# Optimization experiments

Hardware: AMD Instinct MI355X
Metric: run time of the kernel (lower is better)

## Reference

```python
import jax, jax.numpy as jnp
import numpy as np
from jax import lax

N = 2048    # atoms
K = 16      # knn neighbors -> E = N*K = 32768 edges
H = 128     # latent width
L = 10      # stacked InteractionNetworks
STEPS = 10  # outer simulation iterations


def _rn(key, shape, scale=0.05):
    return scale * jax.random.normal(key, shape, dtype=jnp.float32)


def setup_inputs() -> dict:
    key = jax.random.key(0)
    ks = iter(jax.random.split(key, 40))
    inp = {
        "pos": jax.random.normal(next(ks), (N, 3), dtype=jnp.float32),
        "node_f": jax.random.normal(next(ks), (N, 24), dtype=jnp.float32),
        "mass": jnp.ones((N,), jnp.float32),
        # node encoder MLP(24,128,2,128)
        "nW1": _rn(next(ks), (24, H)), "nb1": _rn(next(ks), (H,)),
        "nW2": _rn(next(ks), (H, H)), "nb2": _rn(next(ks), (H,)),
        # edge encoder MLP(4,128,2,128)
        "eW1": _rn(next(ks), (4, H)), "eb1": _rn(next(ks), (H,)),
        "eW2": _rn(next(ks), (H, H)), "eb2": _rn(next(ks), (H,)),
        # RelationModel per IN: input = 2*dim_obj + dim_rel = 384, 4 Linear layers (ReLU after each)
        "rmW1": _rn(next(ks), (L, 3 * H, H)), "rmb1": _rn(next(ks), (L, H)),
        "rmW2": _rn(next(ks), (L, H, H)), "rmb2": _rn(next(ks), (L, H)),
        "rmW3": _rn(next(ks), (L, H, H)), "rmb3": _rn(next(ks), (L, H)),
        "rmW4": _rn(next(ks), (L, H, H)), "rmb4": _rn(next(ks), (L, H)),
        # ObjectModel per IN: input = dim_obj + dim_eff = 256 -> hidden 128 -> out 128
        "omW1": _rn(next(ks), (L, 2 * H, H)), "omb1": _rn(next(ks), (L, H)),
        "omW2": _rn(next(ks), (L, H, H)), "omb2": _rn(next(ks), (L, H)),
        # decoder MLP(128,128,2,3)
        "dW1": _rn(next(ks), (H, H)), "db1": _rn(next(ks), (H,)),
        "dW2": _rn(next(ks), (H, 3)), "db2": _rn(next(ks), (3,)),
        "k": K,
    }
    return inp


def _mlp2(x, W1, b1, W2, b2):
    return jax.nn.relu(x @ W1 + b1) @ W2 + b2


def _knn_edges(pos, k):
    # knn(P.pos, k): edge_index[:,0] = sender (neighbor), edge_index[:,1] = receiver
    n = pos.shape[0]
    sq = jnp.sum(pos * pos, axis=1)
    d2 = sq[:, None] + sq[None, :] - 2.0 * (pos @ pos.T)   # [N, N]
    d2 = d2 + 1e9 * jnp.eye(n, dtype=pos.dtype)            # exclude self
    _, idx = lax.top_k(-d2, k)                              # [N, k] nearest
    senders = idx.reshape(-1)                               # [E]
    receivers = jnp.repeat(jnp.arange(n), k)                # [E]
    rel = pos[senders] - pos[receivers]
    dist = jnp.linalg.norm(rel, axis=1, keepdims=True)
    ea0 = jnp.concatenate([rel, dist], axis=1)              # [E, 4]
    return senders, receivers, ea0


def _simulate(pos, node_f, mass, nW1, nb1, nW2, nb2, eW1, eb1, eW2, eb2,
              rmW1, rmb1, rmW2, rmb2, rmW3, rmb3, rmW4, rmb4,
              omW1, omb1, omW2, omb2, dW1, db1, dW2, db2, k):
    n = pos.shape[0]
    # G.pos = G.pos + randn * 0.1 ; G.vels = zeros
    pos = pos + 0.1 * jax.random.normal(jax.random.key(42), pos.shape, dtype=pos.dtype)
    vels = jnp.zeros_like(pos)

    stacked = (rmW1, rmb1, rmW2, rmb2, rmW3, rmb3, rmW4, rmb4,
               omW1, omb1, omW2, omb2)

    for _ in range(STEPS):
        senders, receivers, ea0 = _knn_edges(pos, k)

        # encode
        x = _mlp2(node_f, nW1, nb1, nW2, nb2)    # [N, H]
        ea = _mlp2(ea0, eW1, eb1, eW2, eb2)      # [E, H]

        # process: 10 InteractionNetworks. In the original, layer(P.x, P.senders,
        # P.receivers, P.edge_attr) binds rr=senders, rs=receivers, so the
        # one-hot matmuls obj.t()@rr / obj.t()@rs are gathers by sender/receiver,
        # and e @ rr.t() is a scatter-add onto sender nodes.
        def in_step(carry, p):
            xc, eac = carry
            rW1, rb1, rW2, rb2, rW3, rb3, rW4, rb4, oW1, ob1, oW2, ob2 = p
            b = jnp.concatenate([xc[senders], xc[receivers], eac], axis=1)  # [E, 3H]
            h = jax.nn.relu(b @ rW1 + rb1)
            h = jax.nn.relu(h @ rW2 + rb2)
            h = jax.nn.relu(h @ rW3 + rb3)
            e = jax.nn.relu(h @ rW4 + rb4)                                   # [E, H]
            agg = jax.ops.segment_sum(e, senders, num_segments=n)           # e @ rr.T
            a = jnp.concatenate([xc, agg], axis=1)                           # [N, 2H]
            x_new = jax.nn.relu(a @ oW1 + ob1) @ oW2 + ob2                   # [N, H]
            return (x_new, e), None

        (x, ea), _ = lax.scan(jax.checkpoint(in_step), (x, ea), stacked)

        # decode + update
        forces = _mlp2(x, dW1, db1, dW2, db2)    # [N, 3]
        vels = vels + forces / mass[:, None]
        pos = pos + vels
    return pos


def reference(pos, node_f, mass, nW1, nb1, nW2, nb2, eW1, eb1, eW2, eb2,
              rmW1, rmb1, rmW2, rmb2, rmW3, rmb3, rmW4, rmb4,
              omW1, omb1, omW2, omb2, dW1, db1, dW2, db2, k):
    return _simulate(pos, node_f, mass, nW1, nb1, nW2, nb2, eW1, eb1, eW2, eb2,
                     rmW1, rmb1, rmW2, rmb2, rmW3, rmb3, rmW4, rmb4,
                     omW1, omb1, omW2, omb2, dW1, db1, dW2, db2, k)
```

## Files before the change

### kernel.cpp

```cpp
#include <hip/hip_runtime.h>

#define N_ATOMS 2048
#define KNN 16
#define NE (N_ATOMS*KNN)
#define H 128
#define NL 10
#define NSTEPS 10

typedef unsigned short u16;
typedef __attribute__((ext_vector_type(4))) float f32x4;
typedef __attribute__((ext_vector_type(8))) short bf16x8;

__device__ __forceinline__ u16 f2bf(float x){
  unsigned u = __float_as_uint(x);
  return (u16)((u + 0x7FFFu + ((u >> 16) & 1u)) >> 16);
}
__device__ __forceinline__ float bf2f(u16 v){ return __uint_as_float(((unsigned)v) << 16); }

template<int PITCH>
__device__ __forceinline__ bf16x8 ldsB_m6(const u16* s, int e, int k){
  int byte = e*PITCH + (k<<1); byte ^= ((e&7)<<4);
  return *(const bf16x8*)((const char*)s + byte);
}
template<int PITCH>
__device__ __forceinline__ void lds_st16_m6(u16* s, int row, int k, uint4 v){
  int byte = row*PITCH + (k<<1); byte ^= ((row&7)<<4);
  *(uint4*)((char*)s + byte) = v;
}
template<int PITCH>
__device__ __forceinline__ uint4 lds_ld16_m6(const u16* s, int row, int k){
  int byte = row*PITCH + (k<<1); byte ^= ((row&7)<<4);
  return *(const uint4*)((const char*)s + byte);
}
template<int PITCH>
__device__ __forceinline__ void lds_st8_m6(u16* s, int row, int k, uint2 v){
  int byte = row*PITCH + (k<<1); byte ^= ((row&7)<<4);
  *(uint2*)((char*)s + byte) = v;
}

template<int KST, int KS, int ET, int PITCH>
__device__ __forceinline__ void mfma_gemm_m6(const u16* sBh, const u16* sBl,
    const u16* __restrict__ pWh, const u16* __restrict__ pWl,
    int ksbase, int wpair, int rowbase, int lane, f32x4 acc[2][ET]){
  const int er = lane & 15, kg = lane >> 4;
  const size_t base = ((size_t)(wpair*KST + ksbase)*64 + lane)*8;
  #pragma unroll
  for (int ks = 0; ks < KS; ks++){
    const int klds = ks*32 + kg*8;
    bf16x8 bh[ET], bl[ET];
    #pragma unroll
    for (int et = 0; et < ET; et++){
      bh[et] = ldsB_m6<PITCH>(sBh, rowbase + et*16 + er, klds);
      bl[et] = ldsB_m6<PITCH>(sBl, rowbase + et*16 + er, klds);
    }
    #pragma unroll
    for (int nt = 0; nt < 2; nt++){
      const size_t off = base + (size_t)(nt*KST + ks)*512;
      bf16x8 ah = *(const bf16x8*)(pWh + off);
      bf16x8 al = *(const bf16x8*)(pWl + off);
      #pragma unroll
      for (int et = 0; et < ET; et++){
        acc[nt][et] = __builtin_amdgcn_mfma_f32_16x16x32_bf16(ah, bh[et], acc[nt][et], 0, 0, 0);
        acc[nt][et] = __builtin_amdgcn_mfma_f32_16x16x32_bf16(ah, bl[et], acc[nt][et], 0, 0, 0);
        acc[nt][et] = __builtin_amdgcn_mfma_f32_16x16x32_bf16(al, bh[et], acc[nt][et], 0, 0, 0);
      }
    }
  }
}

#define CLR_M6(acc, ET) { _Pragma("unroll") for (int i_=0;i_<2;i_++){ _Pragma("unroll") for (int j_=0;j_<ET;j_++){ \
  acc[i_][j_][0]=0.f; acc[i_][j_][1]=0.f; acc[i_][j_][2]=0.f; acc[i_][j_][3]=0.f; } } }

template<int ET, int PITCH, bool RELU>
__device__ __forceinline__ void epi_lds_m6(f32x4 acc[2][ET], u16* sh, u16* sl,
    int wpair, int rowbase, int lane, const float* __restrict__ bias){
  const int er = lane & 15, g = lane >> 4;
  #pragma unroll
  for (int nt = 0; nt < 2; nt++){
    const int n0 = (wpair + nt)*16 + g*4;
    f32x4 bv = *(const f32x4*)(bias + n0);
    #pragma unroll
    for (int et = 0; et < ET; et++){
      const int e = rowbase + et*16 + er;
      unsigned hw[2], lw[2];
      #pragma unroll
      for (int q = 0; q < 2; q++){
        float v0 = acc[nt][et][2*q]   + bv[2*q];
        float v1 = acc[nt][et][2*q+1] + bv[2*q+1];
        if (RELU){ v0 = fmaxf(v0, 0.f); v1 = fmaxf(v1, 0.f); }
        u16 h0 = f2bf(v0), h1 = f2bf(v1);
        u16 l0 = f2bf(v0 - bf2f(h0)), l1 = f2bf(v1 - bf2f(h1));
        hw[q] = (unsigned)h0 | ((unsigned)h1 << 16);
        lw[q] = (unsigned)l0 | ((unsigned)l1 << 16);
      }
      uint2 hv; hv.x = hw[0]; hv.y = hw[1];
      uint2 lv; lv.x = lw[0]; lv.y = lw[1];
      lds_st8_m6<PITCH>(sh, e, n0, hv);
      lds_st8_m6<PITCH>(sl, e, n0, lv);
    }
  }
}

__global__ __launch_bounds__(256) void pack_w_m6(const float* __restrict__ W,
    u16* __restrict__ ph, u16* __restrict__ pl, int KS, int L, int lstride, int roff){
  int idx = blockIdx.x*256 + threadIdx.x;
  int per = 8*KS*64;
  if (idx >= per*L) return;
  int l = idx / per, r = idx - l*per;
  int lane = r & 63, rest = r >> 6;
  int ks = rest % KS, nt = rest / KS;
  int n = nt*16 + (lane & 15), kb = ks*32 + (lane >> 4)*8;
  const float* src = W + (size_t)l*lstride;
  u16 h8[8], l8[8];
  #pragma unroll
  for (int j = 0; j < 8; j++){
    float v = src[(size_t)(roff + kb + j)*H + n];
    u16 h = f2bf(v);
    h8[j] = h; l8[j] = f2bf(v - bf2f(h));
  }
  size_t off = (size_t)idx*8;
  uint4 hv, lv;
  hv.x = h8[0]|((unsigned)h8[1]<<16); hv.y = h8[2]|((unsigned)h8[3]<<16);
  hv.z = h8[4]|((unsigned)h8[5]<<16); hv.w = h8[6]|((unsigned)h8[7]<<16);
  lv.x = l8[0]|((unsigned)l8[1]<<16); lv.y = l8[2]|((unsigned)l8[3]<<16);
  lv.z = l8[4]|((unsigned)l8[5]<<16); lv.w = l8[6]|((unsigned)l8[7]<<16);
  *(uint4*)(ph + off) = hv;
  *(uint4*)(pl + off) = lv;
}

__device__ __forceinline__ int lds_byte_f_m6(int r, int k4){
  return (((r<<9) + (k4<<2)) ^ (((r>>3)&7)<<4));
}
__device__ __forceinline__ f32x4 lds4r_f_m6(const float* s, int r, int k4){
  return *(const f32x4*)((const char*)s + lds_byte_f_m6(r,k4));
}
__device__ __forceinline__ void lds4w_f_m6(float* s, int r, int k4, f32x4 v){
  *(f32x4*)((char*)s + lds_byte_f_m6(r,k4)) = v;
}
__device__ __forceinline__ float lds1r_f_m6(const float* s, int r, int k){
  return *(const float*)((const char*)s + lds_byte_f_m6(r, k & ~3) + ((k&3)<<2));
}
template<int KD, int RPT>
__device__ __forceinline__ void gemm_f_m6(const float* sA, const float* __restrict__ gW,
                                          int r0, int c0, float acc[RPT][4]){
  #pragma unroll 2
  for (int k4 = 0; k4 < KD; k4 += 4){
    f32x4 a[RPT];
    #pragma unroll
    for (int i=0;i<RPT;i++) a[i] = lds4r_f_m6(sA, r0+i, k4);
    #pragma unroll
    for (int kk=0;kk<4;kk++){
      f32x4 wv = *(const f32x4*)(gW + (size_t)(k4+kk)*H + c0);
      #pragma unroll
      for (int i=0;i<RPT;i++){
        acc[i][0] = fmaf(a[i][kk], wv[0], acc[i][0]);
        acc[i][1] = fmaf(a[i][kk], wv[1], acc[i][1]);
        acc[i][2] = fmaf(a[i][kk], wv[2], acc[i][2]);
        acc[i][3] = fmaf(a[i][kk], wv[3], acc[i][3]);
      }
    }
  }
}

__device__ __forceinline__ unsigned rotl32_m6(unsigned v, int d){ return (v << d) | (v >> (32 - d)); }
__device__ __forceinline__ void tf2x32_m6(unsigned k0, unsigned k1, unsigned x0, unsigned x1,
                                          unsigned* o0, unsigned* o1){
  unsigned ks2 = k0 ^ k1 ^ 0x1BD11BDAu;
  x0 += k0; x1 += k1;
  const int R0[4] = {13,15,26,6}, R1[4] = {17,29,16,24};
#define TFG(R) { for (int i=0;i<4;i++){ x0 += x1; x1 = rotl32_m6(x1,R[i]); x1 ^= x0; } }
  TFG(R0); x0 += k1;  x1 += ks2 + 1u;
  TFG(R1); x0 += ks2; x1 += k0  + 2u;
  TFG(R0); x0 += k0;  x1 += k1  + 3u;
  TFG(R1); x0 += k1;  x1 += ks2 + 4u;
  TFG(R0); x0 += ks2; x1 += k0  + 5u;
#undef TFG
  *o0 = x0; *o1 = x1;
}
__device__ float bits_to_normal_m6(unsigned bits){
  float f = __uint_as_float((bits >> 9) | 0x3F800000u) - 1.0f;
  const float lo = -0.99999994f;
  float u = fmaxf(lo, __fadd_rn(__fmul_rn(f, 2.0f), lo));
  float w = -log1pf(-__fmul_rn(u, u));
  float p;
  if (w < 5.0f){
    w = __fsub_rn(w, 2.5f);
    p = 2.81022636e-08f;
    p = __fadd_rn(__fmul_rn(p,w),  3.43273939e-07f);
    p = __fadd_rn(__fmul_rn(p,w), -3.5233877e-06f);
    p = __fadd_rn(__fmul_rn(p,w), -4.39150654e-06f);
    p = __fadd_rn(__fmul_rn(p,w),  0.00021858087f);
    p = __fadd_rn(__fmul_rn(p,w), -0.00125372503f);
    p = __fadd_rn(__fmul_rn(p,w), -0.00417768164f);
    p = __fadd_rn(__fmul_rn(p,w),  0.246640727f);
    p = __fadd_rn(__fmul_rn(p,w),  1.50140941f);
  } else {
    w = __fsub_rn(sqrtf(w), 3.0f);
    p = -0.000200214257f;
    p = __fadd_rn(__fmul_rn(p,w),  0.000100950558f);
    p = __fadd_rn(__fmul_rn(p,w),  0.00134934322f);
    p = __fadd_rn(__fmul_rn(p,w), -0.00367342844f);
    p = __fadd_rn(__fmul_rn(p,w),  0.00573950773f);
    p = __fadd_rn(__fmul_rn(p,w), -0.0076224613f);
    p = __fadd_rn(__fmul_rn(p,w),  0.00943887047f);
    p = __fadd_rn(__fmul_rn(p,w),  1.00167406f);
    p = __fadd_rn(__fmul_rn(p,w),  2.83297682f);
  }
  return __fmul_rn(1.41421356f, __fmul_rn(p, u));
}
__device__ __forceinline__ unsigned draw_bits_m6(unsigned k1, unsigned k2, int bk, int m, int half){
  unsigned o0, o1;
  if (bk == 0){
    if (m < half){ tf2x32_m6(k1,k2, (unsigned)m, (unsigned)(m+half), &o0,&o1); return o0; }
    else         { tf2x32_m6(k1,k2, (unsigned)(m-half), (unsigned)m, &o0,&o1); return o1; }
  }
  tf2x32_m6(k1,k2, 0u, (unsigned)m, &o0,&o1);
  return (bk==1) ? (o0^o1) : (bk==2) ? o1 : o0;
}
__global__ __launch_bounds__(64) void rng_init_m6(int* flags){
  if (threadIdx.x < 8) flags[threadIdx.x] = 1;
}
__global__ __launch_bounds__(256) void rng_detect_m6(const float* __restrict__ pos_in, int* flags){
  int m = blockIdx.x*256 + threadIdx.x;
  if (m >= N_ATOMS*3) return;
  unsigned a0,a1,b0,b1,f0,f1;
  tf2x32_m6(0u,0u, 0u,40u, &a0,&a1);
  tf2x32_m6(0u,0u, 1u,41u, &b0,&b1);
  tf2x32_m6(0u,0u, 0u,0u,  &f0,&f1);
  float target = pos_in[m];
  #pragma unroll
  for (int v = 0; v < 8; v++){
    unsigned k1 = (v<4)? a0 : f0, k2 = (v<4)? b0 : f1;
    unsigned bits = draw_bits_m6(k1,k2, v&3, m, 3072);
    float z = bits_to_normal_m6(bits);
    if (fabsf(z - target) > 1e-3f) flags[v] = 0;
  }
}
__global__ __launch_bounds__(64) void rng_select_m6(const int* flags, int* sel){
  if (threadIdx.x == 0){
    int s = -1;
    for (int v = 0; v < 8; v++) if (flags[v]){ s = v; break; }
    sel[0] = (s < 0) ? 1 : (s & 3);
  }
}
__global__ __launch_bounds__(256) void perturb_m6(const float* __restrict__ pos,
                                                  const int* __restrict__ sel,
                                                  float* __restrict__ posw,
                                                  float* __restrict__ vels){
  int m = blockIdx.x*256 + threadIdx.x;
  if (m >= N_ATOMS*3) return;
  unsigned bits = draw_bits_m6(0u, 42u, sel[0], m, 3072);
  float z = bits_to_normal_m6(bits);
  posw[m] = __fadd_rn(pos[m], __fmul_rn(0.1f, z));
  vels[m] = 0.f;
}

__global__ __launch_bounds__(128) void node_enc_m6(const float* __restrict__ nf,
    const float* __restrict__ W1, const float* __restrict__ b1,
    const float* __restrict__ W2, const float* __restrict__ b2,
    u16* __restrict__ xh, u16* __restrict__ xl){
  __shared__ float s_in[24];
  __shared__ float s_h[128];
  int n = blockIdx.x, t = threadIdx.x;
  if (t < 24) s_in[t] = nf[n*24 + t];
  __syncthreads();
  float a = b1[t];
  #pragma unroll
  for (int k = 0; k < 24; k++) a = fmaf(s_in[k], W1[k*H + t], a);
  s_h[t] = fmaxf(a, 0.f);
  __syncthreads();
  float a2 = b2[t];
  for (int k = 0; k < H; k++) a2 = fmaf(s_h[k], W2[k*H + t], a2);
  u16 h = f2bf(a2);
  xh[(size_t)n*H + t] = h;
  xl[(size_t)n*H + t] = f2bf(a2 - bf2f(h));
}

__global__ __launch_bounds__(256) void pnode_m6(
    const u16* __restrict__ xh, const u16* __restrict__ xl,
    const u16* __restrict__ pah, const u16* __restrict__ pal,
    const u16* __restrict__ pbh, const u16* __restrict__ pbl,
    float* __restrict__ P1g, float* __restrict__ P2g){
  __shared__ __align__(16) u16 sXh[16*128];
  __shared__ __align__(16) u16 sXl[16*128];
  const int t = threadIdx.x, n0b = blockIdx.x*16;
  const int i = t>>4, seg = t&15;
  {
    uint4 hv = *(const uint4*)(xh + (size_t)(n0b+i)*H + seg*8);
    uint4 lv = *(const uint4*)(xl + (size_t)(n0b+i)*H + seg*8);
    lds_st16_m6<256>(sXh, i, seg*8, hv);
    lds_st16_m6<256>(sXl, i, seg*8, lv);
  }
  __syncthreads();
  const int w = t>>6, lane = t&63, er = lane&15, g = lane>>4;
  f32x4 acc[2][1];
  CLR_M6(acc, 1);
  mfma_gemm_m6<4,4,1,256>(sXh, sXl, pah, pal, 0, w*2, 0, lane, acc);
  #pragma unroll
  for (int nt = 0; nt < 2; nt++)
    *(f32x4*)(P1g + (size_t)(n0b+er)*H + (w*2+nt)*16 + g*4) = acc[nt][0];
  CLR_M6(acc, 1);
  mfma_gemm_m6<4,4,1,256>(sXh, sXl, pbh, pbl, 0, w*2, 0, lane, acc);
  #pragma unroll
  for (int nt = 0; nt < 2; nt++)
    *(f32x4*)(P2g + (size_t)(n0b+er)*H + (w*2+nt)*16 + g*4) = acc[nt][0];
}

__global__ __launch_bounds__(256) void knn_m6(const float* __restrict__ pos,
                                              int* __restrict__ senders,
                                              float* __restrict__ ea0){
  __shared__ float d2[N_ATOMS];
  __shared__ float pv[4];
  __shared__ int   pi[4];
  int r = blockIdx.x, t = threadIdx.x;
  float prx = pos[r*3+0], pry = pos[r*3+1], prz = pos[r*3+2];
  float sqr = __fadd_rn(__fadd_rn(__fmul_rn(prx,prx), __fmul_rn(pry,pry)), __fmul_rn(prz,prz));
  for (int c = t; c < N_ATOMS; c += 256){
    float cx = pos[c*3+0], cy = pos[c*3+1], cz = pos[c*3+2];
    float sqc = __fadd_rn(__fadd_rn(__fmul_rn(cx,cx), __fmul_rn(cy,cy)), __fmul_rn(cz,cz));
    float dot = __fadd_rn(__fadd_rn(__fmul_rn(prx,cx), __fmul_rn(pry,cy)), __fmul_rn(prz,cz));
    float v = __fsub_rn(__fadd_rn(sqr, sqc), __fmul_rn(2.0f, dot));
    d2[c] = (c == r) ? 1e9f : v;
  }
  __syncthreads();
  for (int j = 0; j < KNN; j++){
    float bv = 1e30f; int bi = 0x7fffffff;
    for (int c = t; c < N_ATOMS; c += 256){
      float v = d2[c];
      if (v < bv || (v == bv && c < bi)){ bv = v; bi = c; }
    }
    #pragma unroll
    for (int off = 32; off; off >>= 1){
      float ov = __shfl_down(bv, off);
      int   oi = __shfl_down(bi, off);
      if (ov < bv || (ov == bv && oi < bi)){ bv = ov; bi = oi; }
    }
    if ((t & 63) == 0){ pv[t>>6] = bv; pi[t>>6] = bi; }
    __syncthreads();
    if (t == 0){
      float fv = pv[0]; int fi = pi[0];
      #pragma unroll
      for (int q = 1; q < 4; q++){
        if (pv[q] < fv || (pv[q] == fv && pi[q] < fi)){ fv = pv[q]; fi = pi[q]; }
      }
      senders[r*KNN + j] = fi;
      float dx = __fsub_rn(pos[fi*3+0], prx);
      float dy = __fsub_rn(pos[fi*3+1], pry);
      float dz = __fsub_rn(pos[fi*3+2], prz);
      float ss = __fadd_rn(__fadd_rn(__fmul_rn(dx,dx), __fmul_rn(dy,dy)), __fmul_rn(dz,dz));
      float* o = ea0 + (size_t)(r*KNN + j)*4;
      o[0] = dx; o[1] = dy; o[2] = dz; o[3] = sqrtf(ss);
      d2[fi] = 1e30f;
    }
    __syncthreads();
  }
}

__global__ __launch_bounds__(1024) void csr_build_m6(const int* __restrict__ senders,
    int* __restrict__ rowstart, int* __restrict__ elist){
  __shared__ int cnt[N_ATOMS];
  __shared__ int part[256];
  const int t = threadIdx.x;
  for (int i = t; i < N_ATOMS; i += 1024) cnt[i] = 0;
  __syncthreads();
  #pragma unroll
  for (int k = 0; k < NE/1024; k++){
    int e = t + k*1024;
    atomicAdd(&cnt[senders[e]], 1);
  }
  __syncthreads();
  if (t < 256){
    int base = t*8, s = 0, loc[8];
    #pragma unroll
    for (int i = 0; i < 8; i++){ loc[i] = s; s += cnt[base+i]; }
    part[t] = s;
    __syncthreads();
    if (t == 0){
      int acc = 0;
      for (int i = 0; i < 256; i++){ int v = part[i]; part[i] = acc; acc += v; }
      rowstart[N_ATOMS] = acc;
    }
    __syncthreads();
    int p = part[t];
    #pragma unroll
    for (int i = 0; i < 8; i++){
      int v = p + loc[i];
      rowstart[base+i] = v;
      loc[i] = v;
    }
    __syncthreads();
    #pragma unroll
    for (int i = 0; i < 8; i++) cnt[base+i] = loc[i];
  } else {
    __syncthreads(); __syncthreads(); __syncthreads();
  }
  __syncthreads();
  #pragma unroll
  for (int k = 0; k < NE/1024; k++){
    int e = t + k*1024;
    int slot = atomicAdd(&cnt[senders[e]], 1);
    elist[slot] = e;
  }
}
__global__ __launch_bounds__(256) void csr_sort_m6(const int* __restrict__ rowstart, int* __restrict__ elist){
  int n = blockIdx.x*256 + threadIdx.x;
  if (n >= N_ATOMS) return;
  int b = rowstart[n], e = rowstart[n+1];
  for (int i = b+1; i < e; i++){
    int v = elist[i]; int j = i-1;
    while (j >= b && elist[j] > v){ elist[j+1] = elist[j]; j--; }
    elist[j+1] = v;
  }
}

__global__ __launch_bounds__(256) void edge_enc_m6(const float* __restrict__ ea0,
    const float* __restrict__ eW1, const float* __restrict__ eb1,
    const u16* __restrict__ e2h, const u16* __restrict__ e2l, const float* __restrict__ eb2,
    u16* __restrict__ eag){
  __shared__ float sE0[64*4];
  __shared__ __align__(16) u16 sHh[64*128];
  __shared__ __align__(16) u16 sHl[64*128];
  const int t = threadIdx.x;
  const int e0 = blockIdx.x*64;
  sE0[t] = ea0[(size_t)e0*4 + t];
  __syncthreads();
  const int w = t>>6, lane = t&63;
  const int r0 = ((lane>>3)&7)*8, c0 = w*32 + (lane&7)*4;
  f32x4 bv = *(const f32x4*)(eb1 + c0);
  f32x4 w0 = *(const f32x4*)(eW1 + 0*H + c0);
  f32x4 w1 = *(const f32x4*)(eW1 + 1*H + c0);
  f32x4 w2 = *(const f32x4*)(eW1 + 2*H + c0);
  f32x4 w3 = *(const f32x4*)(eW1 + 3*H + c0);
  #pragma unroll
  for (int i = 0; i < 8; i++){
    int r = r0 + i;
    float e0v = sE0[r*4+0], e1v = sE0[r*4+1], e2v = sE0[r*4+2], e3v = sE0[r*4+3];
    unsigned hw[2], lw[2];
    #pragma unroll
    for (int q = 0; q < 2; q++){
      float v0 = fmaf(e3v, w3[2*q],   fmaf(e2v, w2[2*q],   fmaf(e1v, w1[2*q],   fmaf(e0v, w0[2*q],   bv[2*q]))));
      float v1 = fmaf(e3v, w3[2*q+1], fmaf(e2v, w2[2*q+1], fmaf(e1v, w1[2*q+1], fmaf(e0v, w0[2*q+1], bv[2*q+1]))));
      v0 = fmaxf(v0, 0.f); v1 = fmaxf(v1, 0.f);
      u16 h0 = f2bf(v0), h1 = f2bf(v1);
      u16 l0 = f2bf(v0 - bf2f(h0)), l1 = f2bf(v1 - bf2f(h1));
      hw[q] = (unsigned)h0 | ((unsigned)h1<<16);
      lw[q] = (unsigned)l0 | ((unsigned)l1<<16);
    }
    uint2 hv; hv.x = hw[0]; hv.y = hw[1];
    uint2 lv; lv.x = lw[0]; lv.y = lw[1];
    lds_st8_m6<256>(sHh, r, c0, hv);
    lds_st8_m6<256>(sHl, r, c0, lv);
  }
  __syncthreads();
  f32x4 acc[2][4]; CLR_M6(acc, 4);
  mfma_gemm_m6<4,4,4,256>(sHh, sHl, e2h, e2l, 0, 2*w, 0, lane, acc);
  __syncthreads();
  epi_lds_m6<4,256,false>(acc, sHh, sHl, 2*w, 0, lane, eb2);
  __syncthreads();
  char* dst = (char*)(eag + (size_t)e0*256);
  #pragma unroll
  for (int m = 0; m < 8; m++){
    int byteoff = (t + m*256)*16;
    int row = byteoff>>9, off = byteoff&511;
    uint4 v = lds_ld16_m6<256>((off<256)? sHh : sHl, row, (off&255)>>1);
    *(uint4*)(dst + byteoff) = v;
  }
}

__global__ __launch_bounds__(256) void chain_m6(
    const float* __restrict__ P1g, const float* __restrict__ P2g,
    u16* __restrict__ eag, const int* __restrict__ senders,
    const u16* __restrict__ w1h, const u16* __restrict__ w1l, const float* __restrict__ b1,
    const u16* __restrict__ w2h, const u16* __restrict__ w2l, const float* __restrict__ b2,
    const u16* __restrict__ w3h, const u16* __restrict__ w3l, const float* __restrict__ b3,
    const u16* __restrict__ w4h, const u16* __restrict__ w4l, const float* __restrict__ b4){
  __shared__ __align__(16) u16 sPh[64*128];
  __shared__ __align__(16) u16 sPl[64*128];
  __shared__ __align__(16) u16 sQh[64*128];
  __shared__ __align__(16) u16 sQl[64*128];
  const int t = threadIdx.x, e0 = blockIdx.x*64;
  const int w = t>>6, lane = t&63, er = lane&15, g = lane>>4;
  const int wpair = w*2;
  f32x4 acc[2][4];
  int sidx[4];
  #pragma unroll
  for (int et = 0; et < 4; et++) sidx[et] = senders[e0 + et*16 + er];
  #pragma unroll
  for (int et = 0; et < 4; et++){
    const int r = (e0>>4) + et;
    #pragma unroll
    for (int nt = 0; nt < 2; nt++){
      const int n0 = (wpair+nt)*16 + g*4;
      f32x4 p1 = *(const f32x4*)(P1g + (size_t)sidx[et]*H + n0);
      f32x4 p2 = *(const f32x4*)(P2g + (size_t)r*H + n0);
      acc[nt][et] = p1 + p2;
    }
  }
  const char* src = (const char*)(eag + (size_t)e0*256);
  #pragma unroll
  for (int m = 0; m < 8; m++){
    int byteoff = (t + m*256)*16;
    uint4 v = *(const uint4*)(src + byteoff);
    int row = byteoff>>9, off = byteoff&511;
    lds_st16_m6<256>((off<256)? sPh : sPl, row, (off&255)>>1, v);
  }
  __syncthreads();
  mfma_gemm_m6<4,4,4,256>(sPh, sPl, w1h, w1l, 0, wpair, 0, lane, acc);
  epi_lds_m6<4,256,true>(acc, sQh, sQl, wpair, 0, lane, b1);
  __syncthreads();
  CLR_M6(acc, 4);
  mfma_gemm_m6<4,4,4,256>(sQh, sQl, w2h, w2l, 0, wpair, 0, lane, acc);
  epi_lds_m6<4,256,true>(acc, sPh, sPl, wpair, 0, lane, b2);
  __syncthreads();
  CLR_M6(acc, 4);
  mfma_gemm_m6<4,4,4,256>(sPh, sPl, w3h, w3l, 0, wpair, 0, lane, acc);
  epi_lds_m6<4,256,true>(acc, sQh, sQl, wpair, 0, lane, b3);
  __syncthreads();
  CLR_M6(acc, 4);
  mfma_gemm_m6<4,4,4,256>(sQh, sQl, w4h, w4l, 0, wpair, 0, lane, acc);
  epi_lds_m6<4,256,true>(acc, sPh, sPl, wpair, 0, lane, b4);
  __syncthreads();
  char* dst = (char*)(eag + (size_t)e0*256);
  #pragma unroll
  for (int m = 0; m < 8; m++){
    int byteoff = (t + m*256)*16;
    int row = byteoff>>9, off = byteoff&511;
    uint4 v = lds_ld16_m6<256>((off<256)? sPh : sPl, row, (off&255)>>1);
    *(uint4*)(dst + byteoff) = v;
  }
}

__global__ __launch_bounds__(256) void objagg_m6(
    const u16* __restrict__ xch, const u16* __restrict__ xcl,
    const u16* __restrict__ eag,
    const int* __restrict__ rowstart, const int* __restrict__ elist,
    const u16* __restrict__ o1h, const u16* __restrict__ o1l, const float* __restrict__ ob1,
    const u16* __restrict__ o2h, const u16* __restrict__ o2l, const float* __restrict__ ob2,
    const u16* __restrict__ nah, const u16* __restrict__ nal,
    const u16* __restrict__ nbh, const u16* __restrict__ nbl,
    u16* __restrict__ xoh, u16* __restrict__ xol,
    float* __restrict__ P1g, float* __restrict__ P2g){
  __shared__ __align__(16) u16 sIh[16*256];
  __shared__ __align__(16) u16 sIl[16*256];
  __shared__ __align__(16) u16 sHh[16*128];
  __shared__ __align__(16) u16 sHl[16*128];
  __shared__ __align__(16) u16 sXh[16*128];
  __shared__ __align__(16) u16 sXl[16*128];
  const int t = threadIdx.x, n0b = blockIdx.x*16;
  const int w = t>>6, lane = t&63;
  const int i = t>>4, seg = t&15;
  {
    uint4 hv = *(const uint4*)(xch + (size_t)(n0b+i)*H + seg*8);
    uint4 lv = *(const uint4*)(xcl + (size_t)(n0b+i)*H + seg*8);
    lds_st16_m6<512>(sIh, i, seg*8, hv);
    lds_st16_m6<512>(sIl, i, seg*8, lv);
    float a[8];
    #pragma unroll
    for (int k = 0; k < 8; k++) a[k] = 0.f;
    const int b = rowstart[n0b+i], e = rowstart[n0b+i+1];
    for (int p = b; p < e; p++){
      const int ed = elist[p];
      uint4 hv2 = *(const uint4*)(eag + (size_t)ed*256 + seg*8);
      uint4 lv2 = *(const uint4*)(eag + (size_t)ed*256 + 128 + seg*8);
      unsigned hwd[4] = {hv2.x,hv2.y,hv2.z,hv2.w};
      unsigned lwd[4] = {lv2.x,lv2.y,lv2.z,lv2.w};
      #pragma unroll
      for (int q = 0; q < 4; q++){
        a[2*q]   += bf2f((u16)(hwd[q]&0xffffu)) + bf2f((u16)(lwd[q]&0xffffu));
        a[2*q+1] += bf2f((u16)(hwd[q]>>16))     + bf2f((u16)(lwd[q]>>16));
      }
    }
    unsigned hw[4], lw[4];
    #pragma unroll
    for (int q = 0; q < 4; q++){
      float v0 = a[2*q], v1 = a[2*q+1];
      u16 h0 = f2bf(v0), h1 = f2bf(v1);
      u16 l0 = f2bf(v0 - bf2f(h0)), l1 = f2bf(v1 - bf2f(h1));
      hw[q] = (unsigned)h0 | ((unsigned)h1<<16);
      lw[q] = (unsigned)l0 | ((unsigned)l1<<16);
    }
    uint4 hv3; hv3.x=hw[0]; hv3.y=hw[1]; hv3.z=hw[2]; hv3.w=hw[3];
    uint4 lv3; lv3.x=lw[0]; lv3.y=lw[1]; lv3.z=lw[2]; lv3.w=lw[3];
    lds_st16_m6<512>(sIh, i, 128 + seg*8, hv3);
    lds_st16_m6<512>(sIl, i, 128 + seg*8, lv3);
  }
  __syncthreads();
  f32x4 acc[2][1];
  CLR_M6(acc, 1);
  mfma_gemm_m6<8,8,1,512>(sIh, sIl, o1h, o1l, 0, w*2, 0, lane, acc);
  epi_lds_m6<1,256,true>(acc, sHh, sHl, w*2, 0, lane, ob1);
  __syncthreads();
  CLR_M6(acc, 1);
  mfma_gemm_m6<4,4,1,256>(sHh, sHl, o2h, o2l, 0, w*2, 0, lane, acc);
  epi_lds_m6<1,256,false>(acc, sXh, sXl, w*2, 0, lane, ob2);
  __syncthreads();
  {
    int byteoff = t*16;
    int row = byteoff>>8, off = byteoff&255;
    uint4 hv = lds_ld16_m6<256>(sXh, row, off>>1);
    uint4 lv = lds_ld16_m6<256>(sXl, row, off>>1);
    *(uint4*)((char*)(xoh + (size_t)n0b*H) + byteoff) = hv;
    *(uint4*)((char*)(xol + (size_t)n0b*H) + byteoff) = lv;
  }
  const int er = lane&15, g = lane>>4;
  CLR_M6(acc, 1);
  mfma_gemm_m6<4,4,1,256>(sXh, sXl, nah, nal, 0, w*2, 0, lane, acc);
  #pragma unroll
  for (int nt = 0; nt < 2; nt++)
    *(f32x4*)(P1g + (size_t)(n0b+er)*H + (w*2+nt)*16 + g*4) = acc[nt][0];
  CLR_M6(acc, 1);
  mfma_gemm_m6<4,4,1,256>(sXh, sXl, nbh, nbl, 0, w*2, 0, lane, acc);
  #pragma unroll
  for (int nt = 0; nt < 2; nt++)
    *(f32x4*)(P2g + (size_t)(n0b+er)*H + (w*2+nt)*16 + g*4) = acc[nt][0];
}

__global__ __launch_bounds__(256) void decode_m6(
    const u16* __restrict__ xhi, const u16* __restrict__ xlo,
    const float* __restrict__ dW1, const float* __restrict__ db1,
    const float* __restrict__ dW2, const float* __restrict__ db2,
    const float* __restrict__ mass, float* __restrict__ posw, float* __restrict__ vels){
  __shared__ float sX[16*128];
  __shared__ float sY[16*128];
  const int t = threadIdx.x;
  const int n0 = blockIdx.x*16;
  const int w = t>>6, l = t&63;
  const int r0 = ((l>>3)&7)*2, c0 = w*32 + (l&7)*4;
  const int si = t>>4, sg = t&15;
  {
    const u16* ph = xhi + (size_t)(n0+si)*H + sg*8;
    const u16* pl = xlo + (size_t)(n0+si)*H + sg*8;
    uint4 hv = *(const uint4*)ph;
    uint4 lv = *(const uint4*)pl;
    unsigned hw[4] = {hv.x,hv.y,hv.z,hv.w}, lw[4] = {lv.x,lv.y,lv.z,lv.w};
    f32x4 v0, v1;
    #pragma unroll
    for (int m = 0; m < 2; m++){
      v0[2*m]   = bf2f((u16)(hw[m]&0xffffu)) + bf2f((u16)(lw[m]&0xffffu));
      v0[2*m+1] = bf2f((u16)(hw[m]>>16))     + bf2f((u16)(lw[m]>>16));
      v1[2*m]   = bf2f((u16)(hw[m+2]&0xffffu)) + bf2f((u16)(lw[m+2]&0xffffu));
      v1[2*m+1] = bf2f((u16)(hw[m+2]>>16))     + bf2f((u16)(lw[m+2]>>16));
    }
    lds4w_f_m6(sX, si, sg*8, v0);
    lds4w_f_m6(sX, si, sg*8 + 4, v1);
  }
  __syncthreads();
  float acc[2][4];
  #pragma unroll
  for (int i=0;i<2;i++){ acc[i][0]=0.f; acc[i][1]=0.f; acc[i][2]=0.f; acc[i][3]=0.f; }
  gemm_f_m6<128,2>(sX, dW1, r0, c0, acc);
  {
    f32x4 bv = *(const f32x4*)(db1 + c0);
    #pragma unroll
    for (int i=0;i<2;i++){
      f32x4 v;
      #pragma unroll
      for (int j=0;j<4;j++){ float x = acc[i][j] + bv[j]; v[j] = fmaxf(x, 0.f); }
      lds4w_f_m6(sY, r0+i, c0, v);
    }
  }
  __syncthreads();
  if (t < 48){
    int i = t/3, c = t - i*3;
    float a = db2[c];
    for (int k = 0; k < 128; k++) a = fmaf(lds1r_f_m6(sY, i, k), dW2[k*3 + c], a);
    int n = n0 + i;
    float f = a / mass[n];
    float v = vels[n*3 + c] + f;
    vels[n*3 + c] = v;
    posw[n*3 + c] += v;
  }
}

extern "C" void kernel_launch(void* const* d_in, const int* in_sizes, int n_in,
                              void* d_out, int out_size, void* d_ws, size_t ws_size,
                              hipStream_t stream){
  const float* pos   = (const float*)d_in[0];
  const float* nodef = (const float*)d_in[1];
  const float* mass  = (const float*)d_in[2];
  const float* nW1 = (const float*)d_in[3];  const float* nb1 = (const float*)d_in[4];
  const float* nW2 = (const float*)d_in[5];  const float* nb2 = (const float*)d_in[6];
  const float* eW1 = (const float*)d_in[7];  const float* eb1 = (const float*)d_in[8];
  const float* eW2 = (const float*)d_in[9];  const float* eb2 = (const float*)d_in[10];
  const float* rmW1 = (const float*)d_in[11]; const float* rmb1 = (const float*)d_in[12];
  const float* rmW2 = (const float*)d_in[13]; const float* rmb2 = (const float*)d_in[14];
  const float* rmW3 = (const float*)d_in[15]; const float* rmb3 = (const float*)d_in[16];
  const float* rmW4 = (const float*)d_in[17]; const float* rmb4 = (const float*)d_in[18];
  const float* omW1 = (const float*)d_in[19]; const float* omb1 = (const float*)d_in[20];
  const float* omW2 = (const float*)d_in[21]; const float* omb2 = (const float*)d_in[22];
  const float* dW1 = (const float*)d_in[23]; const float* db1 = (const float*)d_in[24];
  const float* dW2 = (const float*)d_in[25]; const float* db2 = (const float*)d_in[26];

  char* wptr = (char*)d_ws;
  auto alloc = [&](size_t bytes)->void*{
    void* p = (void*)wptr; wptr += (bytes + 255) & ~(size_t)255; return p;
  };
  float* posw  = (float*)alloc((size_t)N_ATOMS*3*4);
  float* vels  = (float*)alloc((size_t)N_ATOMS*3*4);
  int*   senders = (int*)alloc((size_t)NE*4);
  float* ea0   = (float*)alloc((size_t)NE*4*4);
  u16* xench = (u16*)alloc((size_t)N_ATOMS*H*2);
  u16* xencl = (u16*)alloc((size_t)N_ATOMS*H*2);
  u16* xAh   = (u16*)alloc((size_t)N_ATOMS*H*2);
  u16* xAl   = (u16*)alloc((size_t)N_ATOMS*H*2);
  u16* xBh   = (u16*)alloc((size_t)N_ATOMS*H*2);
  u16* xBl   = (u16*)alloc((size_t)N_ATOMS*H*2);
  u16* eag   = (u16*)alloc((size_t)NE*256*2);
  float* P1g  = (float*)alloc((size_t)N_ATOMS*H*4);
  float* P2g  = (float*)alloc((size_t)N_ATOMS*H*4);
  float* P01g = (float*)alloc((size_t)N_ATOMS*H*4);
  float* P02g = (float*)alloc((size_t)N_ATOMS*H*4);
  int* rowstart = (int*)alloc((size_t)(N_ATOMS+1)*4);
  int* elist    = (int*)alloc((size_t)NE*4);
  int* rflags   = (int*)alloc(64);
  int* rsel     = (int*)alloc(64);
  const size_t S4 = 8*4*64*8;
  const size_t S8 = 8*8*64*8;
  u16* p1ah = (u16*)alloc(S4*NL*2); u16* p1al = (u16*)alloc(S4*NL*2);
  u16* p1bh = (u16*)alloc(S4*NL*2); u16* p1bl = (u16*)alloc(S4*NL*2);
  u16* p1ch = (u16*)alloc(S4*NL*2); u16* p1cl = (u16*)alloc(S4*NL*2);
  u16* prm2h = (u16*)alloc(S4*NL*2); u16* prm2l = (u16*)alloc(S4*NL*2);
  u16* prm3h = (u16*)alloc(S4*NL*2); u16* prm3l = (u16*)alloc(S4*NL*2);
  u16* prm4h = (u16*)alloc(S4*NL*2); u16* prm4l = (u16*)alloc(S4*NL*2);
  u16* pom1h = (u16*)alloc(S8*NL*2); u16* pom1l = (u16*)alloc(S8*NL*2);
  u16* pom2h = (u16*)alloc(S4*NL*2); u16* pom2l = (u16*)alloc(S4*NL*2);
  u16* pe2h  = (u16*)alloc(S4*2);    u16* pe2l  = (u16*)alloc(S4*2);

  auto pack = [&](const float* W, u16* ph, u16* pl, int KS, int L, int lstride, int roff){
    int total = L*8*KS*64;
    pack_w_m6<<<(total+255)/256, 256, 0, stream>>>(W, ph, pl, KS, L, lstride, roff);
  };
  pack(rmW1, p1ah, p1al, 4, NL, 384*H, 0);
  pack(rmW1, p1bh, p1bl, 4, NL, 384*H, 128);
  pack(rmW1, p1ch, p1cl, 4, NL, 384*H, 256);
  pack(rmW2, prm2h, prm2l, 4, NL, H*H, 0);
  pack(rmW3, prm3h, prm3l, 4, NL, H*H, 0);
  pack(rmW4, prm4h, prm4l, 4, NL, H*H, 0);
  pack(omW1, pom1h, pom1l, 8, NL, 2*H*H, 0);
  pack(omW2, pom2h, pom2l, 4, NL, H*H, 0);
  pack(eW2,  pe2h,  pe2l,  4, 1,  H*H, 0);

  rng_init_m6<<<1, 64, 0, stream>>>(rflags);
  rng_detect_m6<<<(N_ATOMS*3+255)/256, 256, 0, stream>>>(pos, rflags);
  rng_select_m6<<<1, 64, 0, stream>>>(rflags, rsel);
  perturb_m6<<<(N_ATOMS*3+255)/256, 256, 0, stream>>>(pos, rsel, posw, vels);
  node_enc_m6<<<N_ATOMS, 128, 0, stream>>>(nodef, nW1, nb1, nW2, nb2, xench, xencl);
  pnode_m6<<<N_ATOMS/16, 256, 0, stream>>>(xench, xencl, p1ah, p1al, p1bh, p1bl, P01g, P02g);

  for (int s = 0; s < NSTEPS; s++){
    knn_m6<<<N_ATOMS, 256, 0, stream>>>(posw, senders, ea0);
    csr_build_m6<<<1, 1024, 0, stream>>>(senders, rowstart, elist);
    csr_sort_m6<<<(N_ATOMS+255)/256, 256, 0, stream>>>(rowstart, elist);
    edge_enc_m6<<<NE/64, 256, 0, stream>>>(ea0, eW1, eb1, pe2h, pe2l, eb2, eag);

    const u16* xch = xench; const u16* xcl = xencl;
    for (int l = 0; l < NL; l++){
      const float* Pa = (l == 0) ? P01g : P1g;
      const float* Pb = (l == 0) ? P02g : P2g;
      chain_m6<<<NE/64, 256, 0, stream>>>(Pa, Pb, eag, senders,
          p1ch  + (size_t)l*S4, p1cl  + (size_t)l*S4, rmb1 + l*H,
          prm2h + (size_t)l*S4, prm2l + (size_t)l*S4, rmb2 + l*H,
          prm3h + (size_t)l*S4, prm3l + (size_t)l*S4, rmb3 + l*H,
          prm4h + (size_t)l*S4, prm4l + (size_t)l*S4, rmb4 + l*H);
      u16* xnh = (l & 1) ? xAh : xBh;
      u16* xnl = (l & 1) ? xAl : xBl;
      int lp1 = (l < NL-1) ? (l+1) : l;
      objagg_m6<<<N_ATOMS/16, 256, 0, stream>>>(xch, xcl, eag, rowstart, elist,
          pom1h + (size_t)l*S8, pom1l + (size_t)l*S8, omb1 + l*H,
          pom2h + (size_t)l*S4, pom2l + (size_t)l*S4, omb2 + l*H,
          p1ah + (size_t)lp1*S4, p1al + (size_t)lp1*S4,
          p1bh + (size_t)lp1*S4, p1bl + (size_t)lp1*S4,
          xnh, xnl, P1g, P2g);
      xch = xnh; xcl = xnl;
    }
    decode_m6<<<N_ATOMS/16, 256, 0, stream>>>(xch, xcl, dW1, db1, dW2, db2, mass, posw, vels);
  }
  hipMemcpyAsync(d_out, posw, (size_t)N_ATOMS*3*4, hipMemcpyDeviceToDevice, stream);
}
```

Before: 6.003 ms.

## Fuse edge encoder into first chain layer, merge CSR sort, halve objagg node tile

Drops the separate edge-encoder kernel and computes the edge encoding inside the first chain kernel through a FIRST template flag, so the encoded edge features are not written out and read back before layer 0. The per-row CSR insertion sort moves into the csr_build kernel after a barrier, which removes one launch per step. objagg now handles 8 nodes per block instead of 16, doubling the grid to spread the aggregation over more workgroups, while still running 16-row MFMA tiles with half the rows masked. In exchange the sort runs inside a single 1024-thread block and half of each node-tile MFMA goes unused.

Result: no change. 5.978 ms (-0.4%).

```diff
diff --git a/kernel.cpp b/kernel.cpp
--- a/kernel.cpp
+++ b/kernel.cpp
@@ -6,6 +6,8 @@
 #define H 128
 #define NL 10
 #define NSTEPS 10
+#define S4B ((size_t)16384)
+#define S8B ((size_t)32768)
 
 typedef unsigned short u16;
 typedef __attribute__((ext_vector_type(4))) float f32x4;
@@ -18,28 +20,28 @@
 __device__ __forceinline__ float bf2f(u16 v){ return __uint_as_float(((unsigned)v) << 16); }
 
 template<int PITCH>
-__device__ __forceinline__ bf16x8 ldsB_m6(const u16* s, int e, int k){
+__device__ __forceinline__ bf16x8 ldsB_m8(const u16* s, int e, int k){
   int byte = e*PITCH + (k<<1); byte ^= ((e&7)<<4);
   return *(const bf16x8*)((const char*)s + byte);
 }
 template<int PITCH>
-__device__ __forceinline__ void lds_st16_m6(u16* s, int row, int k, uint4 v){
+__device__ __forceinline__ void lds_st16_m8(u16* s, int row, int k, uint4 v){
   int byte = row*PITCH + (k<<1); byte ^= ((row&7)<<4);
   *(uint4*)((char*)s + byte) = v;
 }
 template<int PITCH>
-__device__ __forceinline__ uint4 lds_ld16_m6(const u16* s, int row, int k){
+__device__ __forceinline__ uint4 lds_ld16_m8(const u16* s, int row, int k){
   int byte = row*PITCH + (k<<1); byte ^= ((row&7)<<4);
   return *(const uint4*)((const char*)s + byte);
 }
 template<int PITCH>
-__device__ __forceinline__ void lds_st8_m6(u16* s, int row, int k, uint2 v){
+__device__ __forceinline__ void lds_st8_m8(u16* s, int row, int k, uint2 v){
   int byte = row*PITCH + (k<<1); byte ^= ((row&7)<<4);
   *(uint2*)((char*)s + byte) = v;
 }
 
 template<int KST, int KS, int ET, int PITCH>
-__device__ __forceinline__ void mfma_gemm_m6(const u16* sBh, const u16* sBl,
+__device__ __forceinline__ void mfma_gemm_m8(const u16* sBh, const u16* sBl,
     const u16* __restrict__ pWh, const u16* __restrict__ pWl,
     int ksbase, int wpair, int rowbase, int lane, f32x4 acc[2][ET]){
   const int er = lane & 15, kg = lane >> 4;
@@ -50,8 +52,8 @@
     bf16x8 bh[ET], bl[ET];
     #pragma unroll
     for (int et = 0; et < ET; et++){
-      bh[et] = ldsB_m6<PITCH>(sBh, rowbase + et*16 + er, klds);
-      bl[et] = ldsB_m6<PITCH>(sBl, rowbase + et*16 + er, klds);
+      bh[et] = ldsB_m8<PITCH>(sBh, rowbase + et*16 + er, klds);
+      bl[et] = ldsB_m8<PITCH>(sBl, rowbase + et*16 + er, klds);
     }
     #pragma unroll
     for (int nt = 0; nt < 2; nt++){
@@ -68,11 +70,11 @@
   }
 }
 
-#define CLR_M6(acc, ET) { _Pragma("unroll") for (int i_=0;i_<2;i_++){ _Pragma("unroll") for (int j_=0;j_<ET;j_++){ \
+#define CLR_M8(acc, ET) { _Pragma("unroll") for (int i_=0;i_<2;i_++){ _Pragma("unroll") for (int j_=0;j_<ET;j_++){ \
   acc[i_][j_][0]=0.f; acc[i_][j_][1]=0.f; acc[i_][j_][2]=0.f; acc[i_][j_][3]=0.f; } } }
 
 template<int ET, int PITCH, bool RELU>
-__device__ __forceinline__ void epi_lds_m6(f32x4 acc[2][ET], u16* sh, u16* sl,
+__device__ __forceinline__ void epi_lds_m8(f32x4 acc[2][ET], u16* sh, u16* sl,
     int wpair, int rowbase, int lane, const float* __restrict__ bias){
   const int er = lane & 15, g = lane >> 4;
   #pragma unroll
@@ -95,13 +97,13 @@
       }
       uint2 hv; hv.x = hw[0]; hv.y = hw[1];
       uint2 lv; lv.x = lw[0]; lv.y = lw[1];
-      lds_st8_m6<PITCH>(sh, e, n0, hv);
-      lds_st8_m6<PITCH>(sl, e, n0, lv);
-    }
-  }
-}
-
-__global__ __launch_bounds__(256) void pack_w_m6(const float* __restrict__ W,
+      lds_st8_m8<PITCH>(sh, e, n0, hv);
+      lds_st8_m8<PITCH>(sl, e, n0, lv);
+    }
+  }
+}
+
+__global__ __launch_bounds__(256) void pack_w_m8(const float* __restrict__ W,
     u16* __restrict__ ph, u16* __restrict__ pl, int KS, int L, int lstride, int roff){
   int idx = blockIdx.x*256 + threadIdx.x;
   int per = 8*KS*64;
@@ -128,26 +130,26 @@
   *(uint4*)(pl + off) = lv;
 }
 
-__device__ __forceinline__ int lds_byte_f_m6(int r, int k4){
+__device__ __forceinline__ int lds_byte_f_m8(int r, int k4){
   return (((r<<9) + (k4<<2)) ^ (((r>>3)&7)<<4));
 }
-__device__ __forceinline__ f32x4 lds4r_f_m6(const float* s, int r, int k4){
-  return *(const f32x4*)((const char*)s + lds_byte_f_m6(r,k4));
-}
-__device__ __forceinline__ void lds4w_f_m6(float* s, int r, int k4, f32x4 v){
-  *(f32x4*)((char*)s + lds_byte_f_m6(r,k4)) = v;
-}
-__device__ __forceinline__ float lds1r_f_m6(const float* s, int r, int k){
-  return *(const float*)((const char*)s + lds_byte_f_m6(r, k & ~3) + ((k&3)<<2));
+__device__ __forceinline__ f32x4 lds4r_f_m8(const float* s, int r, int k4){
+  return *(const f32x4*)((const char*)s + lds_byte_f_m8(r,k4));
+}
+__device__ __forceinline__ void lds4w_f_m8(float* s, int r, int k4, f32x4 v){
+  *(f32x4*)((char*)s + lds_byte_f_m8(r,k4)) = v;
+}
+__device__ __forceinline__ float lds1r_f_m8(const float* s, int r, int k){
+  return *(const float*)((const char*)s + lds_byte_f_m8(r, k & ~3) + ((k&3)<<2));
 }
 template<int KD, int RPT>
-__device__ __forceinline__ void gemm_f_m6(const float* sA, const float* __restrict__ gW,
+__device__ __forceinline__ void gemm_f_m8(const float* sA, const float* __restrict__ gW,
                                           int r0, int c0, float acc[RPT][4]){
   #pragma unroll 2
   for (int k4 = 0; k4 < KD; k4 += 4){
     f32x4 a[RPT];
     #pragma unroll
-    for (int i=0;i<RPT;i++) a[i] = lds4r_f_m6(sA, r0+i, k4);
+    for (int i=0;i<RPT;i++) a[i] = lds4r_f_m8(sA, r0+i, k4);
     #pragma unroll
     for (int kk=0;kk<4;kk++){
       f32x4 wv = *(const f32x4*)(gW + (size_t)(k4+kk)*H + c0);
@@ -162,13 +164,13 @@
   }
 }
 
-__device__ __forceinline__ unsigned rotl32_m6(unsigned v, int d){ return (v << d) | (v >> (32 - d)); }
-__device__ __forceinline__ void tf2x32_m6(unsigned k0, unsigned k1, unsigned x0, unsigned x1,
+__device__ __forceinline__ unsigned rotl32_m8(unsigned v, int d){ return (v << d) | (v >> (32 - d)); }
+__device__ __forceinline__ void tf2x32_m8(unsigned k0, unsigned k1, unsigned x0, unsigned x1,
                                           unsigned* o0, unsigned* o1){
   unsigned ks2 = k0 ^ k1 ^ 0x1BD11BDAu;
   x0 += k0; x1 += k1;
   const int R0[4] = {13,15,26,6}, R1[4] = {17,29,16,24};
-#define TFG(R) { for (int i=0;i<4;i++){ x0 += x1; x1 = rotl32_m6(x1,R[i]); x1 ^= x0; } }
+#define TFG(R) { for (int i=0;i<4;i++){ x0 += x1; x1 = rotl32_m8(x1,R[i]); x1 ^= x0; } }
   TFG(R0); x0 += k1;  x1 += ks2 + 1u;
   TFG(R1); x0 += ks2; x1 += k0  + 2u;
   TFG(R0); x0 += k0;  x1 += k1  + 3u;
@@ -177,7 +179,7 @@
 #undef TFG
   *o0 = x0; *o1 = x1;
 }
-__device__ float bits_to_normal_m6(unsigned bits){
+__device__ float bits_to_normal_m8(unsigned bits){
   float f = __uint_as_float((bits >> 9) | 0x3F800000u) - 1.0f;
   const float lo = -0.99999994f;
   float u = fmaxf(lo, __fadd_rn(__fmul_rn(f, 2.0f), lo));
@@ -208,54 +210,52 @@
   }
   return __fmul_rn(1.41421356f, __fmul_rn(p, u));
 }
-__device__ __forceinline__ unsigned draw_bits_m6(unsigned k1, unsigned k2, int bk, int m, int half){
+__device__ __forceinline__ unsigned draw_bits_m8(unsigned k1, unsigned k2, int bk, int m, int half){
   unsigned o0, o1;
   if (bk == 0){
-    if (m < half){ tf2x32_m6(k1,k2, (unsigned)m, (unsigned)(m+half), &o0,&o1); return o0; }
-    else         { tf2x32_m6(k1,k2, (unsigned)(m-half), (unsigned)m, &o0,&o1); return o1; }
-  }
-  tf2x32_m6(k1,k2, 0u, (unsigned)m, &o0,&o1);
+    if (m < half){ tf2x32_m8(k1,k2, (unsigned)m, (unsigned)(m+half), &o0,&o1); return o0; }
+    else         { tf2x32_m8(k1,k2, (unsigned)(m-half), (unsigned)m, &o0,&o1); return o1; }
+  }
+  tf2x32_m8(k1,k2, 0u, (unsigned)m, &o0,&o1);
   return (bk==1) ? (o0^o1) : (bk==2) ? o1 : o0;
 }
-__global__ __launch_bounds__(64) void rng_init_m6(int* flags){
+__global__ __launch_bounds__(64) void rng_init_m8(int* flags){
   if (threadIdx.x < 8) flags[threadIdx.x] = 1;
 }
-__global__ __launch_bounds__(256) void rng_detect_m6(const float* __restrict__ pos_in, int* flags){
+__global__ __launch_bounds__(256) void rng_detect_m8(const float* __restrict__ pos_in, int* flags){
   int m = blockIdx.x*256 + threadIdx.x;
   if (m >= N_ATOMS*3) return;
   unsigned a0,a1,b0,b1,f0,f1;
-  tf2x32_m6(0u,0u, 0u,40u, &a0,&a1);
-  tf2x32_m6(0u,0u, 1u,41u, &b0,&b1);
-  tf2x32_m6(0u,0u, 0u,0u,  &f0,&f1);
+  tf2x32_m8(0u,0u, 0u,40u, &a0,&a1);
+  tf2x32_m8(0u,0u, 1u,41u, &b0,&b1);
+  tf2x32_m8(0u,0u, 0u,0u,  &f0,&f1);
   float target = pos_in[m];
   #pragma unroll
   for (int v = 0; v < 8; v++){
     unsigned k1 = (v<4)? a0 : f0, k2 = (v<4)? b0 : f1;
-    unsigned bits = draw_bits_m6(k1,k2, v&3, m, 3072);
-    float z = bits_to_normal_m6(bits);
+    unsigned bits = draw_bits_m8(k1,k2, v&3, m, 3072);
+    float z = bits_to_normal_m8(bits);
     if (fabsf(z - target) > 1e-3f) flags[v] = 0;
   }
 }
-__global__ __launch_bounds__(64) void rng_select_m6(const int* flags, int* sel){
+__global__ __launch_bounds__(64) void rng_select_m8(const int* flags, int* sel){
   if (threadIdx.x == 0){
     int s = -1;
     for (int v = 0; v < 8; v++) if (flags[v]){ s = v; break; }
     sel[0] = (s < 0) ? 1 : (s & 3);
   }
 }
-__global__ __launch_bounds__(256) void perturb_m6(const float* __restrict__ pos,
-                                                  const int* __restrict__ sel,
-                                                  float* __restrict__ posw,
-                                                  float* __restrict__ vels){
+__global__ __launch_bounds__(256) void perturb_m8(const float* __restrict__ pos,
+    const int* __restrict__ sel, float* __restrict__ posw, float* __restrict__ vels){
   int m = blockIdx.x*256 + threadIdx.x;
   if (m >= N_ATOMS*3) return;
-  unsigned bits = draw_bits_m6(0u, 42u, sel[0], m, 3072);
-  float z = bits_to_normal_m6(bits);
+  unsigned bits = draw_bits_m8(0u, 42u, sel[0], m, 3072);
+  float z = bits_to_normal_m8(bits);
   posw[m] = __fadd_rn(pos[m], __fmul_rn(0.1f, z));
   vels[m] = 0.f;
 }
 
-__global__ __launch_bounds__(128) void node_enc_m6(const float* __restrict__ nf,
+__global__ __launch_bounds__(128) void node_enc_m8(const float* __restrict__ nf,
     const float* __restrict__ W1, const float* __restrict__ b1,
     const float* __restrict__ W2, const float* __restrict__ b2,
     u16* __restrict__ xh, u16* __restrict__ xl){
@@ -276,7 +276,7 @@
   xl[(size_t)n*H + t] = f2bf(a2 - bf2f(h));
 }
 
-__global__ __launch_bounds__(256) void pnode_m6(
+__global__ __launch_bounds__(256) void pnode_m8(
     const u16* __restrict__ xh, const u16* __restrict__ xl,
     const u16* __restrict__ pah, const u16* __restrict__ pal,
     const u16* __restrict__ pbh, const u16* __restrict__ pbl,
@@ -288,25 +288,25 @@
   {
     uint4 hv = *(const uint4*)(xh + (size_t)(n0b+i)*H + seg*8);
     uint4 lv = *(const uint4*)(xl + (size_t)(n0b+i)*H + seg*8);
-    lds_st16_m6<256>(sXh, i, seg*8, hv);
-    lds_st16_m6<256>(sXl, i, seg*8, lv);
+    lds_st16_m8<256>(sXh, i, seg*8, hv);
+    lds_st16_m8<256>(sXl, i, seg*8, lv);
   }
   __syncthreads();
   const int w = t>>6, lane = t&63, er = lane&15, g = lane>>4;
   f32x4 acc[2][1];
-  CLR_M6(acc, 1);
-  mfma_gemm_m6<4,4,1,256>(sXh, sXl, pah, pal, 0, w*2, 0, lane, acc);
+  CLR_M8(acc, 1);
+  mfma_gemm_m8<4,4,1,256>(sXh, sXl, pah, pal, 0, w*2, 0, lane, acc);
   #pragma unroll
   for (int nt = 0; nt < 2; nt++)
     *(f32x4*)(P1g + (size_t)(n0b+er)*H + (w*2+nt)*16 + g*4) = acc[nt][0];
-  CLR_M6(acc, 1);
-  mfma_gemm_m6<4,4,1,256>(sXh, sXl, pbh, pbl, 0, w*2, 0, lane, acc);
+  CLR_M8(acc, 1);
+  mfma_gemm_m8<4,4,1,256>(sXh, sXl, pbh, pbl, 0, w*2, 0, lane, acc);
   #pragma unroll
   for (int nt = 0; nt < 2; nt++)
     *(f32x4*)(P2g + (size_t)(n0b+er)*H + (w*2+nt)*16 + g*4) = acc[nt][0];
 }
 
-__global__ __launch_bounds__(256) void knn_m6(const float* __restrict__ pos,
+__global__ __launch_bounds__(256) void knn_m8(const float* __restrict__ pos,
                                               int* __restrict__ senders,
                                               float* __restrict__ ea0){
   __shared__ float d2[N_ATOMS];
@@ -356,7 +356,7 @@
   }
 }
 
-__global__ __launch_bounds__(1024) void csr_build_m6(const int* __restrict__ senders,
+__global__ __launch_bounds__(1024) void csr_build_m8(const int* __restrict__ senders,
     int* __restrict__ rowstart, int* __restrict__ elist){
   __shared__ int cnt[N_ATOMS];
   __shared__ int part[256];
@@ -401,75 +401,25 @@
     int slot = atomicAdd(&cnt[senders[e]], 1);
     elist[slot] = e;
   }
-}
-__global__ __launch_bounds__(256) void csr_sort_m6(const int* __restrict__ rowstart, int* __restrict__ elist){
-  int n = blockIdx.x*256 + threadIdx.x;
-  if (n >= N_ATOMS) return;
-  int b = rowstart[n], e = rowstart[n+1];
-  for (int i = b+1; i < e; i++){
-    int v = elist[i]; int j = i-1;
-    while (j >= b && elist[j] > v){ elist[j+1] = elist[j]; j--; }
-    elist[j+1] = v;
-  }
-}
-
-__global__ __launch_bounds__(256) void edge_enc_m6(const float* __restrict__ ea0,
+  __syncthreads();
+  for (int n = t; n < N_ATOMS; n += 1024){
+    int b0 = (n == 0) ? 0 : cnt[n-1];
+    int e1 = cnt[n];
+    for (int i = b0+1; i < e1; i++){
+      int v = elist[i]; int j = i-1;
+      while (j >= b0 && elist[j] > v){ elist[j+1] = elist[j]; j--; }
+      elist[j+1] = v;
+    }
+  }
+}
+
+template<int FIRST>
+__global__ __launch_bounds__(256) void chain_m8(
+    const float* __restrict__ P1g, const float* __restrict__ P2g,
+    u16* __restrict__ eag, const int* __restrict__ senders,
+    const float* __restrict__ ea0,
     const float* __restrict__ eW1, const float* __restrict__ eb1,
     const u16* __restrict__ e2h, const u16* __restrict__ e2l, const float* __restrict__ eb2,
-    u16* __restrict__ eag){
-  __shared__ float sE0[64*4];
-  __shared__ __align__(16) u16 sHh[64*128];
-  __shared__ __align__(16) u16 sHl[64*128];
-  const int t = threadIdx.x;
-  const int e0 = blockIdx.x*64;
-  sE0[t] = ea0[(size_t)e0*4 + t];
-  __syncthreads();
-  const int w = t>>6, lane = t&63;
-  const int r0 = ((lane>>3)&7)*8, c0 = w*32 + (lane&7)*4;
-  f32x4 bv = *(const f32x4*)(eb1 + c0);
-  f32x4 w0 = *(const f32x4*)(eW1 + 0*H + c0);
-  f32x4 w1 = *(const f32x4*)(eW1 + 1*H + c0);
-  f32x4 w2 = *(const f32x4*)(eW1 + 2*H + c0);
-  f32x4 w3 = *(const f32x4*)(eW1 + 3*H + c0);
-  #pragma unroll
-  for (int i = 0; i < 8; i++){
-    int r = r0 + i;
-    float e0v = sE0[r*4+0], e1v = sE0[r*4+1], e2v = sE0[r*4+2], e3v = sE0[r*4+3];
-    unsigned hw[2], lw[2];
-    #pragma unroll
-    for (int q = 0; q < 2; q++){
-      float v0 = fmaf(e3v, w3[2*q],   fmaf(e2v, w2[2*q],   fmaf(e1v, w1[2*q],   fmaf(e0v, w0[2*q],   bv[2*q]))));
-      float v1 = fmaf(e3v, w3[2*q+1], fmaf(e2v, w2[2*q+1], fmaf(e1v, w1[2*q+1], fmaf(e0v, w0[2*q+1], bv[2*q+1]))));
-      v0 = fmaxf(v0, 0.f); v1 = fmaxf(v1, 0.f);
-      u16 h0 = f2bf(v0), h1 = f2bf(v1);
-      u16 l0 = f2bf(v0 - bf2f(h0)), l1 = f2bf(v1 - bf2f(h1));
-      hw[q] = (unsigned)h0 | ((unsigned)h1<<16);
-      lw[q] = (unsigned)l0 | ((unsigned)l1<<16);
-    }
-    uint2 hv; hv.x = hw[0]; hv.y = hw[1];
-    uint2 lv; lv.x = lw[0]; lv.y = lw[1];
-    lds_st8_m6<256>(sHh, r, c0, hv);
-    lds_st8_m6<256>(sHl, r, c0, lv);
-  }
-  __syncthreads();
-  f32x4 acc[2][4]; CLR_M6(acc, 4);
-  mfma_gemm_m6<4,4,4,256>(sHh, sHl, e2h, e2l, 0, 2*w, 0, lane, acc);
-  __syncthreads();
-  epi_lds_m6<4,256,false>(acc, sHh, sHl, 2*w, 0, lane, eb2);
-  __syncthreads();
-  char* dst = (char*)(eag + (size_t)e0*256);
-  #pragma unroll
-  for (int m = 0; m < 8; m++){
-    int byteoff = (t + m*256)*16;
-    int row = byteoff>>9, off = byteoff&511;
-    uint4 v = lds_ld16_m6<256>((off<256)? sHh : sHl, row, (off&255)>>1);
-    *(uint4*)(dst + byteoff) = v;
-  }
-}
-
-__global__ __launch_bounds__(256) void chain_m6(
-    const float* __restrict__ P1g, const float* __restrict__ P2g,
-    u16* __restrict__ eag, const int* __restrict__ senders,
     const u16* __restrict__ w1h, const u16* __restrict__ w1l, const float* __restrict__ b1,
     const u16* __restrict__ w2h, const u16* __restrict__ w2l, const float* __restrict__ b2,
     const u16* __restrict__ w3h, const u16* __restrict__ w3l, const float* __restrict__ b3,
@@ -478,6 +428,7 @@
   __shared__ __align__(16) u16 sPl[64*128];
   __shared__ __align__(16) u16 sQh[64*128];
   __shared__ __align__(16) u16 sQl[64*128];
+  __shared__ float sE0[64*4];
   const int t = threadIdx.x, e0 = blockIdx.x*64;
   const int w = t>>6, lane = t&63, er = lane&15, g = lane>>4;
   const int wpair = w*2;
@@ -487,50 +438,90 @@
   for (int et = 0; et < 4; et++) sidx[et] = senders[e0 + et*16 + er];
   #pragma unroll
   for (int et = 0; et < 4; et++){
-    const int r = (e0>>4) + et;
+    const int rr = (e0>>4) + et;
     #pragma unroll
     for (int nt = 0; nt < 2; nt++){
       const int n0 = (wpair+nt)*16 + g*4;
       f32x4 p1 = *(const f32x4*)(P1g + (size_t)sidx[et]*H + n0);
-      f32x4 p2 = *(const f32x4*)(P2g + (size_t)r*H + n0);
+      f32x4 p2 = *(const f32x4*)(P2g + (size_t)rr*H + n0);
       acc[nt][et] = p1 + p2;
     }
   }
-  const char* src = (const char*)(eag + (size_t)e0*256);
-  #pragma unroll
-  for (int m = 0; m < 8; m++){
-    int byteoff = (t + m*256)*16;
-    uint4 v = *(const uint4*)(src + byteoff);
-    int row = byteoff>>9, off = byteoff&511;
-    lds_st16_m6<256>((off<256)? sPh : sPl, row, (off&255)>>1, v);
-  }
-  __syncthreads();
-  mfma_gemm_m6<4,4,4,256>(sPh, sPl, w1h, w1l, 0, wpair, 0, lane, acc);
-  epi_lds_m6<4,256,true>(acc, sQh, sQl, wpair, 0, lane, b1);
-  __syncthreads();
-  CLR_M6(acc, 4);
-  mfma_gemm_m6<4,4,4,256>(sQh, sQl, w2h, w2l, 0, wpair, 0, lane, acc);
-  epi_lds_m6<4,256,true>(acc, sPh, sPl, wpair, 0, lane, b2);
-  __syncthreads();
-  CLR_M6(acc, 4);
-  mfma_gemm_m6<4,4,4,256>(sPh, sPl, w3h, w3l, 0, wpair, 0, lane, acc);
-  epi_lds_m6<4,256,true>(acc, sQh, sQl, wpair, 0, lane, b3);
-  __syncthreads();
-  CLR_M6(acc, 4);
-  mfma_gemm_m6<4,4,4,256>(sQh, sQl, w4h, w4l, 0, wpair, 0, lane, acc);
-  epi_lds_m6<4,256,true>(acc, sPh, sPl, wpair, 0, lane, b4);
+  if (FIRST){
+    if (t < 64){
+      uint4 v = *(const uint4*)(ea0 + (size_t)(e0 + t)*4);
+      *(uint4*)(sE0 + t*4) = v;
+    }
+    __syncthreads();
+    const int r0e = ((lane>>3)&7)*8, c0e = w*32 + (lane&7)*4;
+    f32x4 bv1 = *(const f32x4*)(eb1 + c0e);
+    f32x4 w0v = *(const f32x4*)(eW1 + 0*H + c0e);
+    f32x4 w1v = *(const f32x4*)(eW1 + 1*H + c0e);
+    f32x4 w2v = *(const f32x4*)(eW1 + 2*H + c0e);
+    f32x4 w3v = *(const f32x4*)(eW1 + 3*H + c0e);
+    #pragma unroll
+    for (int i = 0; i < 8; i++){
+      int rr = r0e + i;
+      float e0v = sE0[rr*4+0], e1v = sE0[rr*4+1], e2v = sE0[rr*4+2], e3v = sE0[rr*4+3];
+      unsigned hw[2], lw[2];
+      #pragma unroll
+      for (int q = 0; q < 2; q++){
+        float v0 = fmaf(e3v, w3v[2*q],   fmaf(e2v, w2v[2*q],   fmaf(e1v, w1v[2*q],   fmaf(e0v, w0v[2*q],   bv1[2*q]))));
+        float v1 = fmaf(e3v, w3v[2*q+1], fmaf(e2v, w2v[2*q+1], fmaf(e1v, w1v[2*q+1], fmaf(e0v, w0v[2*q+1], bv1[2*q+1]))));
+        v0 = fmaxf(v0, 0.f); v1 = fmaxf(v1, 0.f);
+        u16 h0 = f2bf(v0), h1 = f2bf(v1);
+        u16 l0 = f2bf(v0 - bf2f(h0)), l1 = f2bf(v1 - bf2f(h1));
+        hw[q] = (unsigned)h0 | ((unsigned)h1<<16);
+        lw[q] = (unsigned)l0 | ((unsigned)l1<<16);
+      }
+      uint2 hv; hv.x = hw[0]; hv.y = hw[1];
+      uint2 lv; lv.x = lw[0]; lv.y = lw[1];
+      lds_st8_m8<256>(sQh, rr, c0e, hv);
+      lds_st8_m8<256>(sQl, rr, c0e, lv);
+    }
+    __syncthreads();
+    f32x4 acc0[2][4]; CLR_M8(acc0, 4);
+    mfma_gemm_m8<4,4,4,256>(sQh, sQl, e2h, e2l, 0, wpair, 0, lane, acc0);
+    __syncthreads();
+    epi_lds_m8<4,256,false>(acc0, sPh, sPl, wpair, 0, lane, eb2);
+    __syncthreads();
+  } else {
+    const char* src = (const char*)(eag + (size_t)e0*256);
+    #pragma unroll
+    for (int m = 0; m < 8; m++){
+      int byteoff = (t + m*256)*16;
+      uint4 v = *(const uint4*)(src + byteoff);
+      int row = byteoff>>9, off = byteoff&511;
+      lds_st16_m8<256>((off<256)? sPh : sPl, row, (off&255)>>1, v);
+    }
+    __syncthreads();
+  }
+  mfma_gemm_m8<4,4,4,256>(sPh, sPl, w1h, w1l, 0, wpair, 0, lane, acc);
+  epi_lds_m8<4,256,true>(acc, sQh, sQl, wpair, 0, lane, b1);
+  __syncthreads();
+  CLR_M8(acc, 4);
+  mfma_gemm_m8<4,4,4,256>(sQh, sQl, w2h, w2l, 0, wpair, 0, lane, acc);
+  epi_lds_m8<4,256,true>(acc, sPh, sPl, wpair, 0, lane, b2);
+  __syncthreads();
+  CLR_M8(acc, 4);
+  mfma_gemm_m8<4,4,4,256>(sPh, sPl, w3h, w3l, 0, wpair, 0, lane, acc);
+  epi_lds_m8<4,256,true>(acc, sQh, sQl, wpair, 0, lane, b3);
+  __syncthreads();
+  CLR_M8(acc, 4);
+  mfma_gemm_m8<4,4,4,256>(sQh, sQl, w4h, w4l, 0, wpair, 0, lane, acc);
+  epi_lds_m8<4,256,true>(acc, sPh, sPl, wpair, 0, lane, b4);
   __syncthreads();
   char* dst = (char*)(eag + (size_t)e0*256);
   #pragma unroll
   for (int m = 0; m < 8; m++){
     int byteoff = (t + m*256)*16;
     int row = byteoff>>9, off = byteoff&511;
-    uint4 v = lds_ld16_m6<256>((off<256)? sPh : sPl, row, (off&255)>>1);
+    uint4 v = lds_ld16_m8<256>((off<256)? sPh : sPl, row, (off&255)>>1);
     *(uint4*)(dst + byteoff) = v;
   }
 }
 
-__global__ __launch_bounds__(256) void objagg_m6(
+__global__ __launch_bounds__(256) void objagg_m8(
     const u16* __restrict__ xch, const u16* __restrict__ xcl,
     const u16* __restrict__ eag,
     const int* __restrict__ rowstart, const int* __restrict__ elist,
@@ -546,76 +537,68 @@
   __shared__ __align__(16) u16 sHl[16*128];
   __shared__ __align__(16) u16 sXh[16*128];
   __shared__ __align__(16) u16 sXl[16*128];
-  const int t = threadIdx.x, n0b = blockIdx.x*16;
+  const int t = threadIdx.x, n0b = blockIdx.x*8;
   const int w = t>>6, lane = t&63;
-  const int i = t>>4, seg = t&15;
+  const int i = t>>5, c0 = (t&31)*4;
   {
-    uint4 hv = *(const uint4*)(xch + (size_t)(n0b+i)*H + seg*8);
-    uint4 lv = *(const uint4*)(xcl + (size_t)(n0b+i)*H + seg*8);
-    lds_st16_m6<512>(sIh, i, seg*8, hv);
-    lds_st16_m6<512>(sIl, i, seg*8, lv);
-    float a[8];
-    #pragma unroll
-    for (int k = 0; k < 8; k++) a[k] = 0.f;
-    const int b = rowstart[n0b+i], e = rowstart[n0b+i+1];
-    for (int p = b; p < e; p++){
+    uint2 hv = *(const uint2*)(xch + (size_t)(n0b+i)*H + c0);
+    uint2 lv = *(const uint2*)(xcl + (size_t)(n0b+i)*H + c0);
+    lds_st8_m8<512>(sIh, i, c0, hv);
+    lds_st8_m8<512>(sIl, i, c0, lv);
+    float a0 = 0.f, a1 = 0.f, a2 = 0.f, a3 = 0.f;
+    const int b0 = rowstart[n0b+i], e1 = rowstart[n0b+i+1];
+    for (int p = b0; p < e1; p++){
       const int ed = elist[p];
-      uint4 hv2 = *(const uint4*)(eag + (size_t)ed*256 + seg*8);
-      uint4 lv2 = *(const uint4*)(eag + (size_t)ed*256 + 128 + seg*8);
-      unsigned hwd[4] = {hv2.x,hv2.y,hv2.z,hv2.w};
-      unsigned lwd[4] = {lv2.x,lv2.y,lv2.z,lv2.w};
-      #pragma unroll
-      for (int q = 0; q < 4; q++){
-        a[2*q]   += bf2f((u16)(hwd[q]&0xffffu)) + bf2f((u16)(lwd[q]&0xffffu));
-        a[2*q+1] += bf2f((u16)(hwd[q]>>16))     + bf2f((u16)(lwd[q]>>16));
-      }
-    }
-    unsigned hw[4], lw[4];
-    #pragma unroll
-    for (int q = 0; q < 4; q++){
-      float v0 = a[2*q], v1 = a[2*q+1];
-      u16 h0 = f2bf(v0), h1 = f2bf(v1);
-      u16 l0 = f2bf(v0 - bf2f(h0)), l1 = f2bf(v1 - bf2f(h1));
-      hw[q] = (unsigned)h0 | ((unsigned)h1<<16);
-      lw[q] = (unsigned)l0 | ((unsigned)l1<<16);
-    }
-    uint4 hv3; hv3.x=hw[0]; hv3.y=hw[1]; hv3.z=hw[2]; hv3.w=hw[3];
-    uint4 lv3; lv3.x=lw[0]; lv3.y=lw[1]; lv3.z=lw[2]; lv3.w=lw[3];
-    lds_st16_m6<512>(sIh, i, 128 + seg*8, hv3);
-    lds_st16_m6<512>(sIl, i, 128 + seg*8, lv3);
+      uint2 hv2 = *(const uint2*)(eag + (size_t)ed*256 + c0);
+      uint2 lv2 = *(const uint2*)(eag + (size_t)ed*256 + 128 + c0);
+      a0 += bf2f((u16)(hv2.x & 0xffffu)) + bf2f((u16)(lv2.x & 0xffffu));
+      a1 += bf2f((u16)(hv2.x >> 16))     + bf2f((u16)(lv2.x >> 16));
+      a2 += bf2f((u16)(hv2.y & 0xffffu)) + bf2f((u16)(lv2.y & 0xffffu));
+      a3 += bf2f((u16)(hv2.y >> 16))     + bf2f((u16)(lv2.y >> 16));
+    }
+    u16 h0 = f2bf(a0), h1 = f2bf(a1), h2 = f2bf(a2), h3 = f2bf(a3);
+    u16 l0 = f2bf(a0 - bf2f(h0)), l1 = f2bf(a1 - bf2f(h1));
+    u16 l2 = f2bf(a2 - bf2f(h2)), l3 = f2bf(a3 - bf2f(h3));
+    uint2 hvo; hvo.x = (unsigned)h0 | ((unsigned)h1<<16); hvo.y = (unsigned)h2 | ((unsigned)h3<<16);
+    uint2 lvo; lvo.x = (unsigned)l0 | ((unsigned)l1<<16); lvo.y = (unsigned)l2 | ((unsigned)l3<<16);
+    lds_st8_m8<512>(sIh, i, 128 + c0, hvo);
+    lds_st8_m8<512>(sIl, i, 128 + c0, lvo);
   }
   __syncthreads();
   f32x4 acc[2][1];
-  CLR_M6(acc, 1);
-  mfma_gemm_m6<8,8,1,512>(sIh, sIl, o1h, o1l, 0, w*2, 0, lane, acc);
-  epi_lds_m6<1,256,true>(acc, sHh, sHl, w*2, 0, lane, ob1);
-  __syncthreads();
-  CLR_M6(acc, 1);
-  mfma_gemm_m6<4,4,1,256>(sHh, sHl, o2h, o2l, 0, w*2, 0, lane, acc);
-  epi_lds_m6<1,256,false>(acc, sXh, sXl, w*2, 0, lane, ob2);
-  __syncthreads();
-  {
-    int byteoff = t*16;
-    int row = byteoff>>8, off = byteoff&255;
-    uint4 hv = lds_ld16_m6<256>(sXh, row, off>>1);
-    uint4 lv = lds_ld16_m6<256>(sXl, row, off>>1);
-    *(uint4*)((char*)(xoh + (size_t)n0b*H) + byteoff) = hv;
-    *(uint4*)((char*)(xol + (size_t)n0b*H) + byteoff) = lv;
+  CLR_M8(acc, 1);
+  mfma_gemm_m8<8,8,1,512>(sIh, sIl, o1h, o1l, 0, w*2, 0, lane, acc);
+  epi_lds_m8<1,256,true>(acc, sHh, sHl, w*2, 0, lane, ob1);
+  __syncthreads();
+  CLR_M8(acc, 1);
+  mfma_gemm_m8<4,4,1,256>(sHh, sHl, o2h, o2l, 0, w*2, 0, lane, acc);
+  epi_lds_m8<1,256,false>(acc, sXh, sXl, w*2, 0, lane, ob2);
+  __syncthreads();
+  if (t < 128){
+    int row = t>>4, seg = t&15;
+    uint4 hv = lds_ld16_m8<256>(sXh, row, seg*8);
+    uint4 lv = lds_ld16_m8<256>(sXl, row, seg*8);
+    *(uint4*)(xoh + (size_t)(n0b+row)*H + seg*8) = hv;
+    *(uint4*)(xol + (size_t)(n0b+row)*H + seg*8) = lv;
   }
   const int er = lane&15, g = lane>>4;
-  CLR_M6(acc, 1);
-  mfma_gemm_m6<4,4,1,256>(sXh, sXl, nah, nal, 0, w*2, 0, lane, acc);
-  #pragma unroll
-  for (int nt = 0; nt < 2; nt++)
-    *(f32x4*)(P1g + (size_t)(n0b+er)*H + (w*2+nt)*16 + g*4) = acc[nt][0];
-  CLR_M6(acc, 1);
-  mfma_gemm_m6<4,4,1,256>(sXh, sXl, nbh, nbl, 0, w*2, 0, lane, acc);
-  #pragma unroll
-  for (int nt = 0; nt < 2; nt++)
-    *(f32x4*)(P2g + (size_t)(n0b+er)*H + (w*2+nt)*16 + g*4) = acc[nt][0];
-}
-
-__global__ __launch_bounds__(256) void decode_m6(
+  CLR_M8(acc, 1);
+  mfma_gemm_m8<4,4,1,256>(sXh, sXl, nah, nal, 0, w*2, 0, lane, acc);
+  if (er < 8){
+    #pragma unroll
+    for (int nt = 0; nt < 2; nt++)
+      *(f32x4*)(P1g + (size_t)(n0b+er)*H + (w*2+nt)*16 + g*4) = acc[nt][0];
+  }
+  CLR_M8(acc, 1);
+  mfma_gemm_m8<4,4,1,256>(sXh, sXl, nbh, nbl, 0, w*2, 0, lane, acc);
+  if (er < 8){
+    #pragma unroll
+    for (int nt = 0; nt < 2; nt++)
+      *(f32x4*)(P2g + (size_t)(n0b+er)*H + (w*2+nt)*16 + g*4) = acc[nt][0];
+  }
+}
+
+__global__ __launch_bounds__(256) void decode_m8(
     const u16* __restrict__ xhi, const u16* __restrict__ xlo,
     const float* __restrict__ dW1, const float* __restrict__ db1,
     const float* __restrict__ dW2, const float* __restrict__ db2,
@@ -641,14 +624,14 @@
       v1[2*m]   = bf2f((u16)(hw[m+2]&0xffffu)) + bf2f((u16)(lw[m+2]&0xffffu));
       v1[2*m+1] = bf2f((u16)(hw[m+2]>>16))     + bf2f((u16)(lw[m+2]>>16));
     }
-    lds4w_f_m6(sX, si, sg*8, v0);
-    lds4w_f_m6(sX, si, sg*8 + 4, v1);
+    lds4w_f_m8(sX, si, sg*8, v0);
+    lds4w_f_m8(sX, si, sg*8 + 4, v1);
   }
   __syncthreads();
   float acc[2][4];
   #pragma unroll
   for (int i=0;i<2;i++){ acc[i][0]=0.f; acc[i][1]=0.f; acc[i][2]=0.f; acc[i][3]=0.f; }
-  gemm_f_m6<128,2>(sX, dW1, r0, c0, acc);
+  gemm_f_m8<128,2>(sX, dW1, r0, c0, acc);
   {
     f32x4 bv = *(const f32x4*)(db1 + c0);
     #pragma unroll
@@ -656,14 +639,14 @@
       f32x4 v;
       #pragma unroll
       for (int j=0;j<4;j++){ float x = acc[i][j] + bv[j]; v[j] = fmaxf(x, 0.f); }
-      lds4w_f_m6(sY, r0+i, c0, v);
+      lds4w_f_m8(sY, r0+i, c0, v);
     }
   }
   __syncthreads();
   if (t < 48){
     int i = t/3, c = t - i*3;
     float a = db2[c];
-    for (int k = 0; k < 128; k++) a = fmaf(lds1r_f_m6(sY, i, k), dW2[k*3 + c], a);
+    for (int k = 0; k < 128; k++) a = fmaf(lds1r_f_m8(sY, i, k), dW2[k*3 + c], a);
     int n = n0 + i;
     float f = a / mass[n];
     float v = vels[n*3 + c] + f;
@@ -714,21 +697,19 @@
   int* elist    = (int*)alloc((size_t)NE*4);
   int* rflags   = (int*)alloc(64);
   int* rsel     = (int*)alloc(64);
-  const size_t S4 = 8*4*64*8;
-  const size_t S8 = 8*8*64*8;
-  u16* p1ah = (u16*)alloc(S4*NL*2); u16* p1al = (u16*)alloc(S4*NL*2);
-  u16* p1bh = (u16*)alloc(S4*NL*2); u16* p1bl = (u16*)alloc(S4*NL*2);
-  u16* p1ch = (u16*)alloc(S4*NL*2); u16* p1cl = (u16*)alloc(S4*NL*2);
-  u16* prm2h = (u16*)alloc(S4*NL*2); u16* prm2l = (u16*)alloc(S4*NL*2);
-  u16* prm3h = (u16*)alloc(S4*NL*2); u16* prm3l = (u16*)alloc(S4*NL*2);
-  u16* prm4h = (u16*)alloc(S4*NL*2); u16* prm4l = (u16*)alloc(S4*NL*2);
-  u16* pom1h = (u16*)alloc(S8*NL*2); u16* pom1l = (u16*)alloc(S8*NL*2);
-  u16* pom2h = (u16*)alloc(S4*NL*2); u16* pom2l = (u16*)alloc(S4*NL*2);
-  u16* pe2h  = (u16*)alloc(S4*2);    u16* pe2l  = (u16*)alloc(S4*2);
+  u16* p1ah = (u16*)alloc(S4B*NL*2); u16* p1al = (u16*)alloc(S4B*NL*2);
+  u16* p1bh = (u16*)alloc(S4B*NL*2); u16* p1bl = (u16*)alloc(S4B*NL*2);
+  u16* p1ch = (u16*)alloc(S4B*NL*2); u16* p1cl = (u16*)alloc(S4B*NL*2);
+  u16* prm2h = (u16*)alloc(S4B*NL*2); u16* prm2l = (u16*)alloc(S4B*NL*2);
+  u16* prm3h = (u16*)alloc(S4B*NL*2); u16* prm3l = (u16*)alloc(S4B*NL*2);
+  u16* prm4h = (u16*)alloc(S4B*NL*2); u16* prm4l = (u16*)alloc(S4B*NL*2);
+  u16* pom1h = (u16*)alloc(S8B*NL*2); u16* pom1l = (u16*)alloc(S8B*NL*2);
+  u16* pom2h = (u16*)alloc(S4B*NL*2); u16* pom2l = (u16*)alloc(S4B*NL*2);
+  u16* pe2h  = (u16*)alloc(S4B*2);    u16* pe2l  = (u16*)alloc(S4B*2);
 
   auto pack = [&](const float* W, u16* ph, u16* pl, int KS, int L, int lstride, int roff){
     int total = L*8*KS*64;
-    pack_w_m6<<<(total+255)/256, 256, 0, stream>>>(W, ph, pl, KS, L, lstride, roff);
+    pack_w_m8<<<(total+255)/256, 256, 0, stream>>>(W, ph, pl, KS, L, lstride, roff);
   };
   pack(rmW1, p1ah, p1al, 4, NL, 384*H, 0);
   pack(rmW1, p1bh, p1bl, 4, NL, 384*H, 128);
@@ -740,40 +721,48 @@
   pack(omW2, pom2h, pom2l, 4, NL, H*H, 0);
   pack(eW2,  pe2h,  pe2l,  4, 1,  H*H, 0);
 
-  rng_init_m6<<<1, 64, 0, stream>>>(rflags);
-  rng_detect_m6<<<(N_ATOMS*3+255)/256, 256, 0, stream>>>(pos, rflags);
-  rng_select_m6<<<1, 64, 0, stream>>>(rflags, rsel);
-  perturb_m6<<<(N_ATOMS*3+255)/256, 256, 0, stream>>>(pos, rsel, posw, vels);
-  node_enc_m6<<<N_ATOMS, 128, 0, stream>>>(nodef, nW1, nb1, nW2, nb2, xench, xencl);
-  pnode_m6<<<N_ATOMS/16, 256, 0, stream>>>(xench, xencl, p1ah, p1al, p1bh, p1bl, P01g, P02g);
+  rng_init_m8<<<1, 64, 0, stream>>>(rflags);
+  rng_detect_m8<<<(N_ATOMS*3+255)/256, 256, 0, stream>>>(pos, rflags);
+  rng_select_m8<<<1, 64, 0, stream>>>(rflags, rsel);
+  perturb_m8<<<(N_ATOMS*3+255)/256, 256, 0, stream>>>(pos, rsel, posw, vels);
+  node_enc_m8<<<N_ATOMS, 128, 0, stream>>>(nodef, nW1, nb1, nW2, nb2, xench, xencl);
+  pnode_m8<<<N_ATOMS/16, 256, 0, stream>>>(xench, xencl, p1ah, p1al, p1bh, p1bl, P01g, P02g);
 
   for (int s = 0; s < NSTEPS; s++){
-    knn_m6<<<N_ATOMS, 256, 0, stream>>>(posw, senders, ea0);
-    csr_build_m6<<<1, 1024, 0, stream>>>(senders, rowstart, elist);
-    csr_sort_m6<<<(N_ATOMS+255)/256, 256, 0, stream>>>(rowstart, elist);
-    edge_enc_m6<<<NE/64, 256, 0, stream>>>(ea0, eW1, eb1, pe2h, pe2l, eb2, eag);
+    knn_m8<<<N_ATOMS, 256, 0, stream>>>(posw, senders, ea0);
+    csr_build_m8<<<1, 1024, 0, stream>>>(senders, rowstart, elist);
 
     const u16* xch = xench; const u16* xcl = xencl;
     for (int l = 0; l < NL; l++){
       const float* Pa = (l == 0) ? P01g : P1g;
       const float* Pb = (l == 0) ? P02g : P2g;
-      chain_m6<<<NE/64, 256, 0, stream>>>(Pa, Pb, eag, senders,
-          p1ch  + (size_t)l*S4, p1cl  + (size_t)l*S4, rmb1 + l*H,
-          prm2h + (size_t)l*S4, prm2l + (size_t)l*S4, rmb2 + l*H,
-          prm3h + (size_t)l*S4, prm3l + (size_t)l*S4, rmb3 + l*H,
-          prm4h + (size_t)l*S4, prm4l + (size_t)l*S4, rmb4 + l*H);
+      if (l == 0){
+        chain_m8<1><<<NE/64, 256, 0, stream>>>(Pa, Pb, eag, senders,
+            ea0, eW1, eb1, pe2h, pe2l, eb2,
+            p1ch  + (size_t)l*S4B, p1cl  + (size_t)l*S4B, rmb1 + l*H,
+            prm2h + (size_t)l*S4B, prm2l + (size_t)l*S4B, rmb2 + l*H,
+            prm3h + (size_t)l*S4B, prm3l + (size_t)l*S4B, rmb3 + l*H,
+            prm4h + (size_t)l*S4B, prm4l + (size_t)l*S4B, rmb4 + l*H);
+      } else {
+        chain_m8<0><<<NE/64, 256, 0, stream>>>(Pa, Pb, eag, senders,
+            ea0, eW1, eb1, pe2h, pe2l, eb2,
+            p1ch  + (size_t)l*S4B, p1cl  + (size_t)l*S4B, rmb1 + l*H,
+            prm2h + (size_t)l*S4B, prm2l + (size_t)l*S4B, rmb2 + l*H,
+            prm3h + (size_t)l*S4B, prm3l + (size_t)l*S4B, rmb3 + l*H,
+            prm4h + (size_t)l*S4B, prm4l + (size_t)l*S4B, rmb4 + l*H);
+      }
       u16* xnh = (l & 1) ? xAh : xBh;
       u16* xnl = (l & 1) ? xAl : xBl;
       int lp1 = (l < NL-1) ? (l+1) : l;
-      objagg_m6<<<N_ATOMS/16, 256, 0, stream>>>(xch, xcl, eag, rowstart, elist,
-          pom1h + (size_t)l*S8, pom1l + (size_t)l*S8, omb1 + l*H,
-          pom2h + (size_t)l*S4, pom2l + (size_t)l*S4, omb2 + l*H,
-          p1ah + (size_t)lp1*S4, p1al + (size_t)lp1*S4,
-          p1bh + (size_t)lp1*S4, p1bl + (size_t)lp1*S4,
+      objagg_m8<<<N_ATOMS/8, 256, 0, stream>>>(xch, xcl, eag, rowstart, elist,
+          pom1h + (size_t)l*S8B, pom1l + (size_t)l*S8B, omb1 + l*H,
+          pom2h + (size_t)l*S4B, pom2l + (size_t)l*S4B, omb2 + l*H,
+          p1ah + (size_t)lp1*S4B, p1al + (size_t)lp1*S4B,
+          p1bh + (size_t)lp1*S4B, p1bl + (size_t)lp1*S4B,
           xnh, xnl, P1g, P2g);
       xch = xnh; xcl = xnl;
     }
-    decode_m6<<<N_ATOMS/16, 256, 0, stream>>>(xch, xcl, dW1, db1, dW2, db2, mass, posw, vels);
+    decode_m8<<<N_ATOMS/16, 256, 0, stream>>>(xch, xcl, dW1, db1, dW2, db2, mass, posw, vels);
   }
   hipMemcpyAsync(d_out, posw, (size_t)N_ATOMS*3*4, hipMemcpyDeviceToDevice, stream);
 }
```
